# Kernel optimization log

Hardware: AMD Instinct MI355X
Metric: run time of the kernel (lower is better)

The kernel has to match this reference:

```python
import jax, jax.numpy as jnp
import numpy as np

B, T, D = 16, 512, 256          # batch, seq_len, d_model (= num features = num graph nodes N)
H, MC, K, DE, DH = 4, 4, 3, 10, 128
GS, SS, AS = 4, 6, 4            # global/sector/asset regime states
TAU = 0.5
STEPS = 3                       # diffusion steps
HID = max(64, D)
DEC_H = max(64, D // 2)


def setup_inputs() -> dict:
    key = jax.random.key(0)
    ks = iter(jax.random.split(key, 64))

    def nrm(shape, s=0.02):
        return (s * jax.random.normal(next(ks), shape)).astype(jnp.float32)

    z = lambda *s: jnp.zeros(s, jnp.float32)
    o = lambda *s: jnp.ones(s, jnp.float32)
    p = dict(
        x=jax.random.normal(next(ks), (B, T, D), dtype=jnp.float32),
        # hierarchical regime controller
        gW1=nrm((D, HID)), gb1=z(HID), g_ln_w=o(HID), g_ln_b=z(HID),
        gW2=nrm((HID, GS)), gb2=z(GS),
        sW1=nrm((D, HID)), sb1=z(HID), sW2=nrm((HID, D * SS)), sb2=z(D * SS),
        aW1=nrm((D, HID)), ab1=z(HID), aW2=nrm((HID, D * AS)), ab2=z(D * AS),
        global_prior=z(GS), sector_prior=z(SS), asset_prior=z(AS),
        g2f=nrm((GS, D)),
        sector_emb=jax.random.normal(next(ks), (SS, D), dtype=jnp.float32),
        asset_emb=jax.random.normal(next(ks), (AS, D), dtype=jnp.float32),
        # bidirectional temporal scan (BI-Mamba stand-in)
        decay_f=nrm((D,), 1.0), decay_b=nrm((D,), 1.0),
        tW=nrm((D, D)), tb=z(D),
        # Bayesian MAGAC + diffusion graph prior
        psi=nrm((H, D, DE), 0.1), log_sigma=jnp.full((H,), -2.0, jnp.float32),
        step_logits=jnp.linspace(-1.0, 0.5, STEPS).astype(jnp.float32),
        noise_scale=jnp.full((STEPS,), 0.05, jnp.float32),
        Wk=nrm((K + 1, T, DH)),
        mean_w=nrm((DH,)), mean_b=z(), lv_w=nrm((DH,)), lv_b=z(),
        # risk-aware decoder
        dW1=nrm((D, DEC_H)), db1=z(DEC_H), d_ln_w=o(DEC_H), d_ln_b=z(DEC_H),
        mW=nrm((DEC_H,)), mb=z(), lvW=nrm((DEC_H,)), lvb=z(),
        cW=nrm((DEC_H,)), cb=z(),
    )
    return p


def _ln(h, w, b):
    m = h.mean(-1, keepdims=True)
    v = h.var(-1, keepdims=True)  # biased, matches torch LayerNorm
    return (h - m) / jnp.sqrt(v + 1e-5) * w + b


def _gelu(h):
    return jax.nn.gelu(h, approximate=False)


def _gumbel_softmax(k, logits):
    u = jax.random.uniform(k, logits.shape, minval=1e-6, maxval=1.0 - 1e-6)
    g = -jnp.log(-jnp.log(u))
    return jax.nn.softmax((logits + g) / TAU, axis=-1)


def _fwd(x, gW1, gb1, g_ln_w, g_ln_b, gW2, gb2, sW1, sb1, sW2, sb2,
         aW1, ab1, aW2, ab2, global_prior, sector_prior, asset_prior,
         g2f, sector_emb, asset_emb, decay_f, decay_b, tW, tb,
         psi, log_sigma, step_logits, noise_scale, Wk,
         mean_w, mean_b, lv_w, lv_b,
         dW1, db1, d_ln_w, d_ln_b, mW, mb, lvW, lvb, cW, cb):
    rk = jax.random.key(42)
    k_g, k_s, k_a, k_eps, k_diff = jax.random.split(rk, 5)

    # ---- hierarchical regime controller ----
    seq_mean = x.mean(1)                               # (B, D)
    diff_summary = (x[:, 1:] - x[:, :-1]).mean(1)      # (B, D)
    g_logits = _gelu(_ln(seq_mean @ gW1 + gb1, g_ln_w, g_ln_b)) @ gW2 + gb2
    s_logits = (_gelu(seq_mean @ sW1 + sb1) @ sW2 + sb2).reshape(B, D, SS)
    a_logits = (_gelu(diff_summary @ aW1 + ab1) @ aW2 + ab2).reshape(B, D, AS)
    g_probs = _gumbel_softmax(k_g, g_logits)
    s_probs = _gumbel_softmax(k_s, s_logits)
    a_probs = _gumbel_softmax(k_a, a_logits)
    global_gate = g_probs @ g2f                                   # (B, D)
    # diagonal of einsum('bfs,sd->bfd') == einsum('bfs,sf->bf')
    sector_gate = jnp.einsum('bfs,sf->bf', s_probs, sector_emb)
    asset_gate = jnp.einsum('bfs,sf->bf', a_probs, asset_emb)
    feature_gate = jax.nn.sigmoid(global_gate + sector_gate + asset_gate)
    gated_x = x * feature_gate[:, None, :]

    # ---- bidirectional temporal EMA scan (BI-Mamba stand-in) ----
    af = jax.nn.sigmoid(decay_f)
    abk = jax.nn.sigmoid(decay_b)
    xs = gated_x.transpose(1, 0, 2)                    # (T, B, D)

    def ema(a):
        def step(h, xt):
            h = a * h + (1.0 - a) * xt
            return h, h
        return step

    _, hf = jax.lax.scan(ema(af), jnp.zeros_like(xs[0]), xs)
    _, hb = jax.lax.scan(ema(abk), jnp.zeros_like(xs[0]), xs[::-1])
    temporal = (hf + hb[::-1]).transpose(1, 0, 2) @ tW + tb       # (B, T, D)
    node_major = temporal.transpose(0, 2, 1)                      # (B, N=D, T)

    # ---- Bayesian adjacency sampling (MC samples per head) ----
    logits = jnp.einsum('hne,hme->hnm', psi, psi) / jnp.sqrt(jnp.float32(DE))
    sigma = jnp.exp(log_sigma)                                    # (H,)
    eps = jax.random.normal(k_eps, (MC, H, D, D))
    A = jax.nn.softmax(logits[None] + sigma[None, :, None, None] * eps, axis=-1)

    # ---- diffusion refinement guided by regime features ----
    ctx = feature_gate.mean(0)
    ctx = ctx / (jnp.linalg.norm(ctx) + 1e-6)
    outer = ctx[:, None] * ctx[None, :]
    outer = outer / jnp.maximum(outer.sum(-1, keepdims=True), 1e-6)
    dkeys = jax.random.split(k_diff, STEPS)
    for s in range(STEPS):                             # fixed small loop, vectorized over (MC,H)
        alpha = jax.nn.sigmoid(step_logits[s])
        noise = noise_scale[s] * jax.random.normal(dkeys[s], A.shape)
        A = alpha * A + (1.0 - alpha) * outer + noise
        A = 0.5 * (A + jnp.swapaxes(A, -1, -2))
        A = jax.nn.softmax(A, axis=-1)

    # ---- K-hop graph conv, averaged over MC samples and heads ----
    Z = jnp.einsum('bnt,td->bnd', node_major, Wk[0])[None, None]  # hop 0
    P = jnp.broadcast_to(node_major, (MC, H, B, D, T))
    for k in range(1, K + 1):
        P = jnp.einsum('mhnp,mhbpt->mhbnt', A, P)
        Z = Z + jnp.einsum('mhbnt,td->mhbnd', P, Wk[k])
    Z = Z.mean((0, 1))                                            # (B, N, DH)
    graph_mean = Z @ mean_w + mean_b                              # (B, N)
    graph_logvar = Z @ lv_w + lv_b                                # (B, N)

    # ---- risk-aware decoder ----
    feat = _ln(_gelu(graph_mean @ dW1 + db1), d_ln_w, d_ln_b)     # (B, DEC_H)
    mean = feat @ mW + mb
    dec_logvar = feat @ lvW + lvb
    _cvar = jax.nn.sigmoid(feat @ cW + cb)  # auxiliary head (not in returned output)
    var = jnp.exp(dec_logvar) + jnp.exp(graph_logvar).sum(1)
    log_var = jnp.log(var)
    return jnp.stack([mean, log_var], axis=-1)                    # (B, 2)


def reference(x, gW1, gb1, g_ln_w, g_ln_b, gW2, gb2, sW1, sb1, sW2, sb2,
              aW1, ab1, aW2, ab2, global_prior, sector_prior, asset_prior,
              g2f, sector_emb, asset_emb, decay_f, decay_b, tW, tb,
              psi, log_sigma, step_logits, noise_scale, Wk,
              mean_w, mean_b, lv_w, lv_b,
              dW1, db1, d_ln_w, d_ln_b, mW, mb, lvW, lvb, cW, cb):
    return _fwd(x, gW1, gb1, g_ln_w, g_ln_b, gW2, gb2, sW1, sb1, sW2, sb2,
                aW1, ab1, aW2, ab2, global_prior, sector_prior, asset_prior,
                g2f, sector_emb, asset_emb, decay_f, decay_b, tW, tb,
                psi, log_sigma, step_logits, noise_scale, Wk,
                mean_w, mean_b, lv_w, lv_b,
                dW1, db1, d_ln_w, d_ln_b, mW, mb, lvW, lvb, cW, cb)
```

## Files before the change

kernel.cpp:

```cpp
#include <hip/hip_runtime.h>
#include <stdint.h>

#define PARTITIONABLE 1

namespace {

constexpr int GSn = 4, SSn = 6, ASn = 4;

struct TFPair { uint32_t a, b; };

__host__ __device__ constexpr uint32_t rotl32(uint32_t x, int d) {
  return (x << d) | (x >> (32 - d));
}

__host__ __device__ constexpr TFPair tf2x32(uint32_t k0, uint32_t k1,
                                            uint32_t x0, uint32_t x1) {
  uint32_t k2 = k0 ^ k1 ^ 0x1BD11BDAu;
  x0 += k0; x1 += k1;
  x0 += x1; x1 = rotl32(x1, 13); x1 ^= x0;
  x0 += x1; x1 = rotl32(x1, 15); x1 ^= x0;
  x0 += x1; x1 = rotl32(x1, 26); x1 ^= x0;
  x0 += x1; x1 = rotl32(x1, 6);  x1 ^= x0;
  x0 += k1; x1 += k2 + 1u;
  x0 += x1; x1 = rotl32(x1, 17); x1 ^= x0;
  x0 += x1; x1 = rotl32(x1, 29); x1 ^= x0;
  x0 += x1; x1 = rotl32(x1, 16); x1 ^= x0;
  x0 += x1; x1 = rotl32(x1, 24); x1 ^= x0;
  x0 += k2; x1 += k0 + 2u;
  x0 += x1; x1 = rotl32(x1, 13); x1 ^= x0;
  x0 += x1; x1 = rotl32(x1, 15); x1 ^= x0;
  x0 += x1; x1 = rotl32(x1, 26); x1 ^= x0;
  x0 += x1; x1 = rotl32(x1, 6);  x1 ^= x0;
  x0 += k0; x1 += k1 + 3u;
  x0 += x1; x1 = rotl32(x1, 17); x1 ^= x0;
  x0 += x1; x1 = rotl32(x1, 29); x1 ^= x0;
  x0 += x1; x1 = rotl32(x1, 16); x1 ^= x0;
  x0 += x1; x1 = rotl32(x1, 24); x1 ^= x0;
  x0 += k1; x1 += k2 + 4u;
  x0 += x1; x1 = rotl32(x1, 13); x1 ^= x0;
  x0 += x1; x1 = rotl32(x1, 15); x1 ^= x0;
  x0 += x1; x1 = rotl32(x1, 26); x1 ^= x0;
  x0 += x1; x1 = rotl32(x1, 6);  x1 ^= x0;
  x0 += k2; x1 += k0 + 5u;
  return TFPair{x0, x1};
}

#if PARTITIONABLE
constexpr TFPair KG  = tf2x32(0u, 42u, 0u, 0u);
constexpr TFPair KS  = tf2x32(0u, 42u, 0u, 1u);
constexpr TFPair KA  = tf2x32(0u, 42u, 0u, 2u);
constexpr TFPair KE  = tf2x32(0u, 42u, 0u, 3u);
constexpr TFPair KD  = tf2x32(0u, 42u, 0u, 4u);
constexpr TFPair DK0 = tf2x32(KD.a, KD.b, 0u, 0u);
constexpr TFPair DK1 = tf2x32(KD.a, KD.b, 0u, 1u);
constexpr TFPair DK2 = tf2x32(KD.a, KD.b, 0u, 2u);
#else
constexpr TFPair SP0 = tf2x32(0u, 42u, 0u, 5u);
constexpr TFPair SP1 = tf2x32(0u, 42u, 1u, 6u);
constexpr TFPair SP2 = tf2x32(0u, 42u, 2u, 7u);
constexpr TFPair SP3 = tf2x32(0u, 42u, 3u, 8u);
constexpr TFPair SP4 = tf2x32(0u, 42u, 4u, 9u);
constexpr TFPair KG  = TFPair{SP0.a, SP1.a};
constexpr TFPair KS  = TFPair{SP2.a, SP3.a};
constexpr TFPair KA  = TFPair{SP4.a, SP0.b};
constexpr TFPair KE  = TFPair{SP1.b, SP2.b};
constexpr TFPair KD  = TFPair{SP3.b, SP4.b};
constexpr TFPair DP0 = tf2x32(KD.a, KD.b, 0u, 3u);
constexpr TFPair DP1 = tf2x32(KD.a, KD.b, 1u, 4u);
constexpr TFPair DP2 = tf2x32(KD.a, KD.b, 2u, 5u);
constexpr TFPair DK0 = TFPair{DP0.a, DP1.a};
constexpr TFPair DK1 = TFPair{DP2.a, DP0.b};
constexpr TFPair DK2 = TFPair{DP1.b, DP2.b};
#endif

__device__ __forceinline__ uint32_t rbits(uint32_t k0, uint32_t k1,
                                          uint32_t idx, uint32_t half) {
#if PARTITIONABLE
  TFPair t = tf2x32(k0, k1, 0u, idx);
  return t.a ^ t.b;
#else
  if (idx < half) return tf2x32(k0, k1, idx, idx + half).a;
  return tf2x32(k0, k1, idx - half, idx).b;
#endif
}

__device__ __forceinline__ float bits_to_u01(uint32_t bits) {
  return __uint_as_float((bits >> 9) | 0x3F800000u) - 1.0f;
}

__device__ __forceinline__ float gumbel_u(uint32_t k0, uint32_t k1,
                                          uint32_t idx, uint32_t half) {
  const float mn = 1e-6f;
  const float mx = 1.0f - 1e-6f;
  float f = bits_to_u01(rbits(k0, k1, idx, half));
  return fmaxf(mn, f * (mx - mn) + mn);
}

__device__ __forceinline__ float erfinv_f32(float x) {
  float w = -log1pf(-x * x);
  float p;
  if (w < 5.0f) {
    w -= 2.5f;
    p = 2.81022636e-08f;
    p = fmaf(p, w, 3.43273939e-07f);
    p = fmaf(p, w, -3.5233877e-06f);
    p = fmaf(p, w, -4.39150654e-06f);
    p = fmaf(p, w, 0.00021858087f);
    p = fmaf(p, w, -0.00125372503f);
    p = fmaf(p, w, -0.00417768164f);
    p = fmaf(p, w, 0.246640727f);
    p = fmaf(p, w, 1.50140941f);
  } else {
    w = sqrtf(w) - 3.0f;
    p = -0.000200214257f;
    p = fmaf(p, w, 0.000100950558f);
    p = fmaf(p, w, 0.00134934322f);
    p = fmaf(p, w, -0.00367342844f);
    p = fmaf(p, w, 0.00573950773f);
    p = fmaf(p, w, -0.0076224613f);
    p = fmaf(p, w, 0.00943887047f);
    p = fmaf(p, w, 1.00167406f);
    p = fmaf(p, w, 2.83297682f);
  }
  return p * x;
}

__device__ __forceinline__ float normal_from(uint32_t k0, uint32_t k1,
                                             uint32_t idx, uint32_t half) {
  const float lo = -0x1.fffffep-1f;
  float f = bits_to_u01(rbits(k0, k1, idx, half));
  float u = fmaxf(lo, f * 2.0f + lo);
  return 1.41421356237f * erfinv_f32(u);
}

__device__ __forceinline__ float gelu_f(float x) {
  return 0.5f * x * (1.0f + erff(x / 1.4142135623730951f));
}
__device__ __forceinline__ float sigmoid_f(float x) {
  return 1.0f / (1.0f + expf(-x));
}

__device__ __forceinline__ float wave_sum(float v) {
  #pragma unroll
  for (int m = 32; m > 0; m >>= 1) v += __shfl_xor(v, m);
  return v;
}
__device__ __forceinline__ float wave_max(float v) {
  #pragma unroll
  for (int m = 32; m > 0; m >>= 1) v = fmaxf(v, __shfl_xor(v, m));
  return v;
}
template <int NW>
__device__ __forceinline__ float blk_sum(float v, float* slots) {
  v = wave_sum(v);
  int wid = threadIdx.x >> 6;
  if ((threadIdx.x & 63) == 0) slots[wid] = v;
  __syncthreads();
  float r = slots[0];
  #pragma unroll
  for (int i = 1; i < NW; ++i) r += slots[i];
  return r;
}
template <int NW>
__device__ __forceinline__ float blk_max(float v, float* slots) {
  v = wave_max(v);
  int wid = threadIdx.x >> 6;
  if ((threadIdx.x & 63) == 0) slots[wid] = v;
  __syncthreads();
  float r = slots[0];
  #pragma unroll
  for (int i = 1; i < NW; ++i) r = fmaxf(r, slots[i]);
  return r;
}


__global__ __launch_bounds__(256) void k_reduce_x(const float* __restrict__ x,
                                                  float* __restrict__ ps) {
  int blk = blockIdx.x;
  int b = blk >> 4, tc = blk & 15;
  int d = threadIdx.x;
  const float* xp = x + ((size_t)b * 512 + tc * 32) * 256 + d;
  float s = 0.f;
  for (int i = 0; i < 32; ++i) s += xp[(size_t)i * 256];
  ps[(size_t)blk * 256 + d] = s;
}

__global__ void k_combine(const float* __restrict__ x,
                          const float* __restrict__ ps, float* __restrict__ sm,
                          float* __restrict__ ds) {
  int b = blockIdx.x, d = threadIdx.x;
  float s = 0.f;
  for (int tc = 0; tc < 16; ++tc) s += ps[(size_t)(b * 16 + tc) * 256 + d];
  sm[b * 256 + d] = s / 512.0f;
  const float* xb = x + (size_t)b * 512 * 256 + d;
  ds[b * 256 + d] = (xb[(size_t)511 * 256] - xb[0]) / 511.0f;
}

__global__ __launch_bounds__(256) void k_hidden(
    const float* __restrict__ sm, const float* __restrict__ ds,
    const float* __restrict__ gW1, const float* __restrict__ gb1,
    const float* __restrict__ glnw, const float* __restrict__ glnb,
    const float* __restrict__ sW1, const float* __restrict__ sb1,
    const float* __restrict__ aW1, const float* __restrict__ ab1,
    float* __restrict__ hgG, float* __restrict__ hgS,
    float* __restrict__ hgA) {
  __shared__ float inv[256];
  __shared__ float s1[4], s2[4];
  int head = blockIdx.x >> 4, b = blockIdx.x & 15, j = threadIdx.x;
  const float* in = (head == 2) ? ds : sm;
  const float* W1 = (head == 0) ? gW1 : (head == 1) ? sW1 : aW1;
  const float* b1 = (head == 0) ? gb1 : (head == 1) ? sb1 : ab1;
  inv[j] = in[b * 256 + j];
  __syncthreads();
  float h = b1[j];
  for (int d = 0; d < 256; ++d) h = fmaf(inv[d], W1[d * 256 + j], h);
  float* outp = (head == 0) ? hgG : (head == 1) ? hgS : hgA;
  if (head == 0) {
    float mean = blk_sum<4>(h, s1) / 256.0f;
    float dv = h - mean;
    float var = blk_sum<4>(dv * dv, s2) / 256.0f;
    h = dv / sqrtf(var + 1e-5f) * glnw[j] + glnb[j];
  }
  outp[b * 256 + j] = gelu_f(h);
}

__global__ __launch_bounds__(192) void k_s2(const float* __restrict__ hgS,
                                            const float* __restrict__ sW2,
                                            const float* __restrict__ sb2,
                                            const float* __restrict__ semb,
                                            float* __restrict__ sgate) {
  __shared__ float hs[256];
  __shared__ float lv[32][6];
  int b = blockIdx.x, f0 = blockIdx.y * 32;
  int tid = threadIdx.x;
  int fl = tid / 6, s = tid - fl * 6;
  for (int i = tid; i < 256; i += 192) hs[i] = hgS[b * 256 + i];
  __syncthreads();
  int f = f0 + fl;
  const float* wcol = sW2 + f * 6 + s;
  float acc = sb2[f * 6 + s];
  for (int d = 0; d < 256; ++d) acc = fmaf(hs[d], wcol[(size_t)d * 1536], acc);
  float u = gumbel_u(KS.a, KS.b, (uint32_t)(b * 256 + f) * 6u + s, 12288u);
  float g = -logf(-logf(u));
  lv[fl][s] = (acc + g) / 0.5f;
  __syncthreads();
  if (tid < 32) {
    int ff = f0 + tid;
    float v0 = lv[tid][0], v1 = lv[tid][1], v2 = lv[tid][2];
    float v3 = lv[tid][3], v4 = lv[tid][4], v5 = lv[tid][5];
    float mx = fmaxf(fmaxf(fmaxf(v0, v1), fmaxf(v2, v3)), fmaxf(v4, v5));
    float e0 = expf(v0 - mx), e1 = expf(v1 - mx), e2 = expf(v2 - mx);
    float e3 = expf(v3 - mx), e4 = expf(v4 - mx), e5 = expf(v5 - mx);
    float sum = e0 + e1 + e2 + e3 + e4 + e5;
    float sg = (e0 * semb[0 * 256 + ff] + e1 * semb[1 * 256 + ff] +
                e2 * semb[2 * 256 + ff] + e3 * semb[3 * 256 + ff] +
                e4 * semb[4 * 256 + ff] + e5 * semb[5 * 256 + ff]) / sum;
    sgate[b * 256 + ff] = sg;
  }
}

__global__ __launch_bounds__(256) void k_a2(const float* __restrict__ hgA,
                                            const float* __restrict__ aW2,
                                            const float* __restrict__ ab2,
                                            const float* __restrict__ aemb,
                                            float* __restrict__ agate) {
  __shared__ float hs[256];
  __shared__ float lv[64][4];
  int b = blockIdx.x, f0 = blockIdx.y * 64;
  int tid = threadIdx.x;
  int fl = tid >> 2, s = tid & 3;
  hs[tid] = hgA[b * 256 + tid];
  __syncthreads();
  int f = f0 + fl;
  const float* wcol = aW2 + f * 4 + s;
  float acc = ab2[f * 4 + s];
  for (int d = 0; d < 256; ++d) acc = fmaf(hs[d], wcol[(size_t)d * 1024], acc);
  float u = gumbel_u(KA.a, KA.b, (uint32_t)(b * 256 + f) * 4u + s, 8192u);
  float g = -logf(-logf(u));
  lv[fl][s] = (acc + g) / 0.5f;
  __syncthreads();
  if (tid < 64) {
    int ff = f0 + tid;
    float v0 = lv[tid][0], v1 = lv[tid][1], v2 = lv[tid][2], v3 = lv[tid][3];
    float mx = fmaxf(fmaxf(v0, v1), fmaxf(v2, v3));
    float e0 = expf(v0 - mx), e1 = expf(v1 - mx);
    float e2 = expf(v2 - mx), e3 = expf(v3 - mx);
    float sum = e0 + e1 + e2 + e3;
    float ag = (e0 * aemb[0 * 256 + ff] + e1 * aemb[1 * 256 + ff] +
                e2 * aemb[2 * 256 + ff] + e3 * aemb[3 * 256 + ff]) / sum;
    agate[b * 256 + ff] = ag;
  }
}

__global__ __launch_bounds__(256) void k_fgate(
    const float* __restrict__ hgG, const float* __restrict__ gW2,
    const float* __restrict__ gb2, const float* __restrict__ g2f,
    const float* __restrict__ sgate, const float* __restrict__ agate,
    float* __restrict__ fg) {
  __shared__ float slots[4][4];
  __shared__ float vals[4];
  __shared__ float gp[4];
  int b = blockIdx.x, j = threadIdx.x;
  float hj = hgG[b * 256 + j];
  float lg[4];
  #pragma unroll
  for (int s = 0; s < 4; ++s)
    lg[s] = blk_sum<4>(hj * gW2[j * 4 + s], slots[s]);
  if (j < 4) {
    float u = gumbel_u(KG.a, KG.b, (uint32_t)(b * 4 + j), 32u);
    float g = -logf(-logf(u));
    vals[j] = (lg[j] + gb2[j] + g) / 0.5f;
  }
  __syncthreads();
  if (j < 4) {
    float mx = fmaxf(fmaxf(vals[0], vals[1]), fmaxf(vals[2], vals[3]));
    float sum = expf(vals[0] - mx) + expf(vals[1] - mx) + expf(vals[2] - mx) +
                expf(vals[3] - mx);
    gp[j] = expf(vals[j] - mx) / sum;
  }
  __syncthreads();
  int f = j;
  float gg = 0.f;
  #pragma unroll
  for (int s = 0; s < 4; ++s) gg = fmaf(gp[s], g2f[s * 256 + f], gg);
  fg[b * 256 + f] = sigmoid_f(gg + sgate[b * 256 + f] + agate[b * 256 + f]);
}

__global__ __launch_bounds__(256) void k_ctx(const float* __restrict__ fg,
                                             float* __restrict__ ctx) {
  __shared__ float s1[4], s2[4];
  int f = threadIdx.x;
  float c = 0.f;
  for (int b = 0; b < 16; ++b) c += fg[b * 256 + f];
  c /= 16.0f;
  float ss = blk_sum<4>(c * c, s1);
  float cv = c / (sqrtf(ss) + 1e-6f);
  ctx[f] = cv;
  float S = blk_sum<4>(cv, s2);
  if (f == 0) ctx[256] = S;
}

__global__ __launch_bounds__(256) void k_vcompute(const float* __restrict__ Wk,
                                                  const float* __restrict__ mean_w,
                                                  const float* __restrict__ lv_w,
                                                  float* __restrict__ v,
                                                  float* __restrict__ sv) {
  int j = blockIdx.x >> 2, tg = blockIdx.x & 3;
  const float* wp = (j & 1) ? lv_w : mean_w;
  const float* Wkk = Wk + (size_t)(j >> 1) * 65536;
  int wid = threadIdx.x >> 6, lane = threadIdx.x & 63;
  float w0 = wp[lane], w1 = wp[64 + lane];
  float svloc = 0.f;
  for (int i = 0; i < 32; ++i) {
    int t = tg * 128 + wid * 32 + i;
    const float* row = Wkk + (size_t)t * 128;
    float s = row[lane] * w0 + row[64 + lane] * w1;
    s = wave_sum(s);
    if (lane == 0) { v[j * 512 + t] = s; svloc += s; }
  }
  if (lane == 0) atomicAdd(&sv[j], svloc);
}

__global__ __launch_bounds__(256) void k_scan1(
    const float* __restrict__ x, const float* __restrict__ fg,
    const float* __restrict__ decay_f, const float* __restrict__ decay_b,
    const float* __restrict__ v, float* __restrict__ Pf, float* __restrict__ Qf,
    float* __restrict__ Pb, float* __restrict__ Qb, float* __restrict__ Lf,
    float* __restrict__ Lb) {
  __shared__ float vv[8][32];
  int blk = blockIdx.x;
  int b = blk >> 4, c = blk & 15;
  int d = threadIdx.x;
  { int j = d >> 5, i = d & 31; vv[j][i] = v[j * 512 + c * 32 + i]; }
  __syncthreads();
  float g = fg[b * 256 + d];
  float af = sigmoid_f(decay_f[d]);
  float ab = sigmoid_f(decay_b[d]);
  float r_gx[32];
  const float* xp = x + ((size_t)b * 512 + c * 32) * 256 + d;
  #pragma unroll
  for (int i = 0; i < 32; ++i) r_gx[i] = xp[(size_t)i * 256] * g;
  float h = 0.f, pw = 1.f;
  float P[8], Q[8];
  #pragma unroll
  for (int j = 0; j < 8; ++j) { P[j] = 0.f; Q[j] = 0.f; }
  #pragma unroll
  for (int i = 0; i < 32; ++i) {
    h = fmaf(af, h, (1.0f - af) * r_gx[i]);
    pw *= af;
    #pragma unroll
    for (int j = 0; j < 8; ++j) {
      float vj = vv[j][i];
      P[j] = fmaf(h, vj, P[j]);
      Q[j] = fmaf(pw, vj, Q[j]);
    }
  }
  size_t base = ((size_t)(b * 16 + c) * 8) * 256 + d;
  #pragma unroll
  for (int j = 0; j < 8; ++j) { Pf[base + j * 256] = P[j]; Qf[base + j * 256] = Q[j]; }
  Lf[(b * 16 + c) * 256 + d] = h;
  h = 0.f; pw = 1.f;
  #pragma unroll
  for (int j = 0; j < 8; ++j) { P[j] = 0.f; Q[j] = 0.f; }
  #pragma unroll
  for (int i = 31; i >= 0; --i) {
    h = fmaf(ab, h, (1.0f - ab) * r_gx[i]);
    pw *= ab;
    #pragma unroll
    for (int j = 0; j < 8; ++j) {
      float vj = vv[j][i];
      P[j] = fmaf(h, vj, P[j]);
      Q[j] = fmaf(pw, vj, Q[j]);
    }
  }
  #pragma unroll
  for (int j = 0; j < 8; ++j) { Pb[base + j * 256] = P[j]; Qb[base + j * 256] = Q[j]; }
  Lb[(b * 16 + c) * 256 + d] = h;
}

__global__ __launch_bounds__(256) void k_scan2(
    const float* __restrict__ Pf, const float* __restrict__ Qf,
    const float* __restrict__ Pb, const float* __restrict__ Qb,
    const float* __restrict__ Lf, const float* __restrict__ Lb,
    const float* __restrict__ decay_f, const float* __restrict__ decay_b,
    float* __restrict__ u) {
  int blk = blockIdx.x;
  int b = blk >> 3, j = blk & 7;
  int d = threadIdx.x;
  float af = sigmoid_f(decay_f[d]);
  float ab = sigmoid_f(decay_b[d]);
  float af32 = af, ab32 = ab;
  #pragma unroll
  for (int q = 0; q < 5; ++q) { af32 *= af32; ab32 *= ab32; }
  float acc = 0.f, H = 0.f;
  for (int c = 0; c < 16; ++c) {
    size_t base = ((size_t)(b * 16 + c) * 8 + j) * 256 + d;
    acc += Pf[base] + H * Qf[base];
    H = Lf[(b * 16 + c) * 256 + d] + af32 * H;
  }
  H = 0.f;
  for (int c = 15; c >= 0; --c) {
    size_t base = ((size_t)(b * 16 + c) * 8 + j) * 256 + d;
    acc += Pb[base] + H * Qb[base];
    H = Lb[(b * 16 + c) * 256 + d] + ab32 * H;
  }
  u[(b * 8 + j) * 256 + d] = acc;
}

__global__ __launch_bounds__(256) void k_ygemm(
    const float* __restrict__ u, const float* __restrict__ tW,
    const float* __restrict__ tb, const float* __restrict__ sv,
    const float* __restrict__ mean_b, const float* __restrict__ lv_b,
    float* __restrict__ gm, float* __restrict__ glv, float* __restrict__ YH) {
  __shared__ float As[32][33];
  __shared__ float Bs[32][33];
  __shared__ float svs[8];
  int n0 = blockIdx.x * 32, m0 = blockIdx.y * 32;
  int tid = threadIdx.x, tx = tid & 31, ty = tid >> 5;
  if (tid < 8) svs[tid] = sv[tid];
  float acc[4] = {0.f, 0.f, 0.f, 0.f};
  for (int k0 = 0; k0 < 256; k0 += 32) {
    #pragma unroll
    for (int l = 0; l < 4; ++l) {
      int e = tid + l * 256, r = e >> 5, cc = e & 31;
      As[r][cc] = u[(size_t)(m0 + r) * 256 + k0 + cc];
      Bs[r][cc] = tW[(size_t)(k0 + r) * 256 + n0 + cc];
    }
    __syncthreads();
    #pragma unroll
    for (int kk = 0; kk < 32; ++kk) {
      float bv = Bs[kk][tx];
      #pragma unroll
      for (int i = 0; i < 4; ++i) acc[i] = fmaf(As[ty + 8 * i][kk], bv, acc[i]);
    }
    __syncthreads();
  }
  int n = n0 + tx;
  float tbn = tb[n];
  float mb0 = mean_b[0], lb0 = lv_b[0];
  #pragma unroll
  for (int i = 0; i < 4; ++i) {
    int row = m0 + ty + 8 * i;
    int b = row >> 3, j = row & 7;
    float val = acc[i] + tbn * svs[j];
    if (j == 0) gm[b * 256 + n] = val + mb0;
    else if (j == 1) glv[b * 256 + n] = val + lb0;
    else {
      int k = (j >> 1) - 1, proj = j & 1;
      YH[k * 8192 + n * 32 + b * 2 + proj] = val;
    }
  }
}

__global__ __launch_bounds__(256) void k_a_init(const float* __restrict__ psi,
                                                const float* __restrict__ log_sigma,
                                                float* __restrict__ A) {
  __shared__ float pn[12];
  __shared__ float s1[4], s2[4];
  int blk = blockIdx.x;
  int mh = blk >> 8, h = mh & 3, n = blk & 255, p = threadIdx.x;
  if (p < 10) pn[p] = psi[(size_t)(h * 256 + n) * 10 + p];
  __syncthreads();
  const float* pp = psi + (size_t)(h * 256 + p) * 10;
  float s = 0.f;
  #pragma unroll
  for (int e = 0; e < 10; ++e) s = fmaf(pn[e], pp[e], s);
  float logit = s / sqrtf(10.0f);
  uint32_t idx = (uint32_t)blk * 256u + (uint32_t)p;
  float eps = normal_from(KE.a, KE.b, idx, 524288u);
  float val = logit + expf(log_sigma[h]) * eps;
  float mx = blk_max<4>(val, s1);
  float e = expf(val - mx);
  float sum = blk_sum<4>(e, s2);
  A[(size_t)blk * 256 + p] = e / sum;
}

__global__ __launch_bounds__(256) void k_mix_sym(
    const float* __restrict__ Ain, float* __restrict__ Aout,
    const float* __restrict__ ctx, const float* __restrict__ step_logits,
    const float* __restrict__ noise_scale, int s, uint32_t dk0, uint32_t dk1) {
  __shared__ float s1[4], s2[4];
  int blk = blockIdx.x;
  int mh = blk >> 8, n = blk & 255, p = threadIdx.x;
  float alpha = sigmoid_f(step_logits[s]);
  float ns = noise_scale[s];
  float cn = ctx[n], cp = ctx[p], S = ctx[256];
  float o_np = (cn * cp) / fmaxf(cn * S, 1e-6f);
  float o_pn = (cp * cn) / fmaxf(cp * S, 1e-6f);
  uint32_t i_np = (uint32_t)blk * 256u + (uint32_t)p;
  uint32_t i_pn = (uint32_t)mh * 65536u + (uint32_t)p * 256u + (uint32_t)n;
  float a_np = Ain[(size_t)mh * 65536 + n * 256 + p];
  float a_pn = Ain[(size_t)mh * 65536 + p * 256 + n];
  float m_np = alpha * a_np + (1.0f - alpha) * o_np +
               ns * normal_from(dk0, dk1, i_np, 524288u);
  float m_pn = alpha * a_pn + (1.0f - alpha) * o_pn +
               ns * normal_from(dk0, dk1, i_pn, 524288u);
  float val = 0.5f * (m_np + m_pn);
  float mx = blk_max<4>(val, s1);
  float e = expf(val - mx);
  float sum = blk_sum<4>(e, s2);
  Aout[(size_t)blk * 256 + p] = e / sum;
}

__global__ __launch_bounds__(256) void k_horner(
    const float* __restrict__ A, const float* __restrict__ Rin, int sRin,
    const float* __restrict__ Yadd, float* __restrict__ Rout) {
  int nt = blockIdx.x, mh = blockIdx.y;
  int n0 = nt * 32;
  __shared__ float As[32][33];
  __shared__ float Bs[32][33];
  int tid = threadIdx.x, tx = tid & 31, ty = tid >> 5;
  float acc[4] = {0.f, 0.f, 0.f, 0.f};
  const float* Ab = A + (size_t)mh * 65536;
  const float* Rb = Rin + (size_t)mh * sRin;
  for (int k0 = 0; k0 < 256; k0 += 32) {
    #pragma unroll
    for (int l = 0; l < 4; ++l) {
      int e = tid + l * 256, r = e >> 5, cc = e & 31;
      As[r][cc] = Ab[(size_t)(n0 + r) * 256 + k0 + cc];
      Bs[r][cc] = Rb[(size_t)(k0 + r) * 32 + cc];
    }
    __syncthreads();
    #pragma unroll
    for (int kk = 0; kk < 32; ++kk) {
      float bv = Bs[kk][tx];
      #pragma unroll
      for (int i = 0; i < 4; ++i) acc[i] = fmaf(As[ty + 8 * i][kk], bv, acc[i]);
    }
    __syncthreads();
  }
  #pragma unroll
  for (int i = 0; i < 4; ++i) {
    int n = n0 + ty + 8 * i;
    float vv = acc[i];
    if (Yadd) vv += Yadd[n * 32 + tx];
    Rout[(size_t)mh * 8192 + (size_t)n * 32 + tx] = vv;
  }
}

__global__ void k_final(const float* __restrict__ R, float* __restrict__ gm,
                        float* __restrict__ glv) {
  int b = blockIdx.x, n = threadIdx.x;
  float sm_ = 0.f, sl = 0.f;
  for (int mh = 0; mh < 16; ++mh) {
    sm_ += R[(size_t)mh * 8192 + n * 32 + b * 2];
    sl += R[(size_t)mh * 8192 + n * 32 + b * 2 + 1];
  }
  gm[b * 256 + n] += sm_ * (1.0f / 16.0f);
  glv[b * 256 + n] += sl * (1.0f / 16.0f);
}

__global__ __launch_bounds__(128) void k_decoder(
    const float* __restrict__ gm, const float* __restrict__ glv,
    const float* __restrict__ dW1, const float* __restrict__ db1,
    const float* __restrict__ dlnw, const float* __restrict__ dlnb,
    const float* __restrict__ mW, const float* __restrict__ mb,
    const float* __restrict__ lvW, const float* __restrict__ lvb,
    float* __restrict__ out) {
  __shared__ float gmv[256];
  __shared__ float s1[2], s2[2], s3[2], s4[2], s5[2];
  int b = blockIdx.x, j = threadIdx.x;
  gmv[j] = gm[b * 256 + j];
  gmv[j + 128] = gm[b * 256 + j + 128];
  __syncthreads();
  float h = db1[j];
  for (int n = 0; n < 256; ++n) h = fmaf(gmv[n], dW1[n * 128 + j], h);
  h = gelu_f(h);
  float mean = blk_sum<2>(h, s1) / 128.0f;
  float dv = h - mean;
  float var = blk_sum<2>(dv * dv, s2) / 128.0f;
  float feat = dv / sqrtf(var + 1e-5f) * dlnw[j] + dlnb[j];
  float m_c = blk_sum<2>(feat * mW[j], s3) + mb[0];
  float lv_c = blk_sum<2>(feat * lvW[j], s4) + lvb[0];
  float se = expf(glv[b * 256 + j]) + expf(glv[b * 256 + j + 128]);
  float sumexp = blk_sum<2>(se, s5);
  if (j == 0) {
    out[b * 2 + 0] = m_c;
    out[b * 2 + 1] = logf(expf(lv_c) + sumexp);
  }
}

constexpr size_t O_SM = 0;
constexpr size_t O_DS = 4096;
constexpr size_t O_PS = 8192;
constexpr size_t O_HGG = 73728;
constexpr size_t O_HGS = 77824;
constexpr size_t O_HGA = 81920;
constexpr size_t O_SG = 86016;
constexpr size_t O_AG = 90112;
constexpr size_t O_FG = 94208;
constexpr size_t O_CTX = 98304;
constexpr size_t O_V = 98624;
constexpr size_t O_SV = 102720;
constexpr size_t O_U = 102784;
constexpr size_t O_PF = 135552;
constexpr size_t O_QF = 659840;
constexpr size_t O_PB = 1184128;
constexpr size_t O_QB = 1708416;
constexpr size_t O_LF = 2232704;
constexpr size_t O_LB = 2298240;
constexpr size_t O_YH = 2363776;
constexpr size_t O_R1 = 2388352;
constexpr size_t O_R2 = 2519424;
constexpr size_t O_GM = 2650496;
constexpr size_t O_GLV = 2654592;
constexpr size_t O_A = 2658688;
constexpr size_t O_A2 = 3707264;

}

extern "C" void kernel_launch(void* const* d_in, const int* in_sizes, int n_in,
                              void* d_out, int out_size, void* d_ws,
                              size_t ws_size, hipStream_t stream) {
  (void)in_sizes; (void)n_in; (void)out_size; (void)ws_size;
  const float* x = (const float*)d_in[0];
  const float* gW1 = (const float*)d_in[1];
  const float* gb1 = (const float*)d_in[2];
  const float* g_ln_w = (const float*)d_in[3];
  const float* g_ln_b = (const float*)d_in[4];
  const float* gW2 = (const float*)d_in[5];
  const float* gb2 = (const float*)d_in[6];
  const float* sW1 = (const float*)d_in[7];
  const float* sb1 = (const float*)d_in[8];
  const float* sW2 = (const float*)d_in[9];
  const float* sb2 = (const float*)d_in[10];
  const float* aW1 = (const float*)d_in[11];
  const float* ab1 = (const float*)d_in[12];
  const float* aW2 = (const float*)d_in[13];
  const float* ab2 = (const float*)d_in[14];
  const float* g2f = (const float*)d_in[18];
  const float* sector_emb = (const float*)d_in[19];
  const float* asset_emb = (const float*)d_in[20];
  const float* decay_f = (const float*)d_in[21];
  const float* decay_b = (const float*)d_in[22];
  const float* tW = (const float*)d_in[23];
  const float* tb = (const float*)d_in[24];
  const float* psi = (const float*)d_in[25];
  const float* log_sigma = (const float*)d_in[26];
  const float* step_logits = (const float*)d_in[27];
  const float* noise_scale = (const float*)d_in[28];
  const float* Wk = (const float*)d_in[29];
  const float* mean_w = (const float*)d_in[30];
  const float* mean_b = (const float*)d_in[31];
  const float* lv_w = (const float*)d_in[32];
  const float* lv_b = (const float*)d_in[33];
  const float* dW1 = (const float*)d_in[34];
  const float* db1 = (const float*)d_in[35];
  const float* d_ln_w = (const float*)d_in[36];
  const float* d_ln_b = (const float*)d_in[37];
  const float* mW = (const float*)d_in[38];
  const float* mb = (const float*)d_in[39];
  const float* lvW = (const float*)d_in[40];
  const float* lvb = (const float*)d_in[41];
  float* out = (float*)d_out;
  float* w = (float*)d_ws;

  const uint32_t dka[3] = {DK0.a, DK1.a, DK2.a};
  const uint32_t dkb[3] = {DK0.b, DK1.b, DK2.b};

  hipMemsetAsync(w + O_SV, 0, 64 * sizeof(float), stream);

  k_reduce_x<<<256, 256, 0, stream>>>(x, w + O_PS);
  k_combine<<<16, 256, 0, stream>>>(x, w + O_PS, w + O_SM, w + O_DS);
  k_hidden<<<48, 256, 0, stream>>>(w + O_SM, w + O_DS, gW1, gb1, g_ln_w,
                                   g_ln_b, sW1, sb1, aW1, ab1, w + O_HGG,
                                   w + O_HGS, w + O_HGA);
  k_s2<<<dim3(16, 8), 192, 0, stream>>>(w + O_HGS, sW2, sb2, sector_emb,
                                        w + O_SG);
  k_a2<<<dim3(16, 4), 256, 0, stream>>>(w + O_HGA, aW2, ab2, asset_emb,
                                        w + O_AG);
  k_fgate<<<16, 256, 0, stream>>>(w + O_HGG, gW2, gb2, g2f, w + O_SG, w + O_AG,
                                  w + O_FG);
  k_ctx<<<1, 256, 0, stream>>>(w + O_FG, w + O_CTX);

  k_a_init<<<4096, 256, 0, stream>>>(psi, log_sigma, w + O_A);
  const size_t asrc[3] = {O_A, O_A2, O_A};
  const size_t adst[3] = {O_A2, O_A, O_A2};
  for (int s = 0; s < 3; ++s) {
    k_mix_sym<<<4096, 256, 0, stream>>>(w + asrc[s], w + adst[s], w + O_CTX,
                                        step_logits, noise_scale, s, dka[s],
                                        dkb[s]);
  }

  k_vcompute<<<32, 256, 0, stream>>>(Wk, mean_w, lv_w, w + O_V, w + O_SV);
  k_scan1<<<256, 256, 0, stream>>>(x, w + O_FG, decay_f, decay_b, w + O_V,
                                   w + O_PF, w + O_QF, w + O_PB, w + O_QB,
                                   w + O_LF, w + O_LB);
  k_scan2<<<128, 256, 0, stream>>>(w + O_PF, w + O_QF, w + O_PB, w + O_QB,
                                   w + O_LF, w + O_LB, decay_f, decay_b,
                                   w + O_U);
  k_ygemm<<<dim3(8, 4), 256, 0, stream>>>(w + O_U, tW, tb, w + O_SV, mean_b,
                                          lv_b, w + O_GM, w + O_GLV, w + O_YH);

  k_horner<<<dim3(8, 16), 256, 0, stream>>>(w + O_A2, w + O_YH + 2 * 8192, 0,
                                            w + O_YH + 1 * 8192, w + O_R1);
  k_horner<<<dim3(8, 16), 256, 0, stream>>>(w + O_A2, w + O_R1, 8192, w + O_YH,
                                            w + O_R2);
  k_horner<<<dim3(8, 16), 256, 0, stream>>>(w + O_A2, w + O_R2, 8192, nullptr,
                                            w + O_R1);
  k_final<<<16, 256, 0, stream>>>(w + O_R1, w + O_GM, w + O_GLV);

  k_decoder<<<16, 128, 0, stream>>>(w + O_GM, w + O_GLV, dW1, db1, d_ln_w,
                                    d_ln_b, mW, mb, lvW, lvb, out);
}
```

Measured before the change: 358.6 us.

## Fuse many small kernels into phased launches with heterogeneous block roles

Restructures the pipeline from about twenty launches into eleven kernels. Each kernel runs several independent phases, chosen by block index (e.g. hidden layer alongside A-init, gates fused with sector/asset heads), and all pointers are passed in a single Params struct. This targets launch overhead and the idle GPU time in tiny serial kernels by overlapping independent work within one grid. The cost is more complex block-to-phase mapping, and possibly more registers or shared memory per kernel.

```diff
diff --git a/kernel.cpp b/kernel.cpp
--- a/kernel.cpp
+++ b/kernel.cpp
@@ -4,8 +4,6 @@
 #define PARTITIONABLE 1
 
 namespace {
-
-constexpr int GSn = 4, SSn = 6, ASn = 4;
 
 struct TFPair { uint32_t a, b; };
 
@@ -173,182 +171,53 @@
   return r;
 }
 
-
-__global__ __launch_bounds__(256) void k_reduce_x(const float* __restrict__ x,
-                                                  float* __restrict__ ps) {
-  int blk = blockIdx.x;
-  int b = blk >> 4, tc = blk & 15;
-  int d = threadIdx.x;
-  const float* xp = x + ((size_t)b * 512 + tc * 32) * 256 + d;
-  float s = 0.f;
-  for (int i = 0; i < 32; ++i) s += xp[(size_t)i * 256];
-  ps[(size_t)blk * 256 + d] = s;
-}
-
-__global__ void k_combine(const float* __restrict__ x,
-                          const float* __restrict__ ps, float* __restrict__ sm,
-                          float* __restrict__ ds) {
-  int b = blockIdx.x, d = threadIdx.x;
-  float s = 0.f;
-  for (int tc = 0; tc < 16; ++tc) s += ps[(size_t)(b * 16 + tc) * 256 + d];
-  sm[b * 256 + d] = s / 512.0f;
-  const float* xb = x + (size_t)b * 512 * 256 + d;
-  ds[b * 256 + d] = (xb[(size_t)511 * 256] - xb[0]) / 511.0f;
-}
-
-__global__ __launch_bounds__(256) void k_hidden(
-    const float* __restrict__ sm, const float* __restrict__ ds,
-    const float* __restrict__ gW1, const float* __restrict__ gb1,
-    const float* __restrict__ glnw, const float* __restrict__ glnb,
-    const float* __restrict__ sW1, const float* __restrict__ sb1,
-    const float* __restrict__ aW1, const float* __restrict__ ab1,
-    float* __restrict__ hgG, float* __restrict__ hgS,
-    float* __restrict__ hgA) {
-  __shared__ float inv[256];
-  __shared__ float s1[4], s2[4];
-  int head = blockIdx.x >> 4, b = blockIdx.x & 15, j = threadIdx.x;
-  const float* in = (head == 2) ? ds : sm;
-  const float* W1 = (head == 0) ? gW1 : (head == 1) ? sW1 : aW1;
-  const float* b1 = (head == 0) ? gb1 : (head == 1) ? sb1 : ab1;
-  inv[j] = in[b * 256 + j];
+struct Params {
+  const float *x, *gW1, *gb1, *glnw, *glnb, *gW2, *gb2, *sW1, *sb1, *sW2, *sb2,
+      *aW1, *ab1, *aW2, *ab2, *g2f, *semb, *aemb, *decay_f, *decay_b, *tW, *tb,
+      *psi, *log_sigma, *step_logits, *noise_scale, *Wk, *mean_w, *mean_b,
+      *lv_w, *lv_b, *dW1, *db1, *dlnw, *dlnb, *mW, *mb, *lvW, *lvb;
+  float* out;
+  float *ps, *ds, *hgG, *hgS, *hgA, *fg, *ctx, *v, *sv, *u, *Pf, *Qf, *Pb, *Qb,
+      *Lf, *Lb, *YH, *R1, *R2, *gm, *glv, *A, *A2;
+};
+
+
+__device__ __forceinline__ void phase_hidden(const Params& P, float* smem,
+                                             int bid, int tid) {
+  float* inv = smem;
+  float* s1 = smem + 256;
+  float* s2 = smem + 260;
+  int head = bid >> 4, b = bid & 15;
+  float iv;
+  if (head < 2) {
+    float s = 0.f;
+    for (int tc = 0; tc < 16; ++tc) s += P.ps[(size_t)(b * 16 + tc) * 256 + tid];
+    iv = s / 512.0f;
+  } else {
+    iv = P.ds[b * 256 + tid];
+  }
+  inv[tid] = iv;
   __syncthreads();
-  float h = b1[j];
-  for (int d = 0; d < 256; ++d) h = fmaf(inv[d], W1[d * 256 + j], h);
-  float* outp = (head == 0) ? hgG : (head == 1) ? hgS : hgA;
+  const float* W1 = (head == 0) ? P.gW1 : (head == 1) ? P.sW1 : P.aW1;
+  const float* b1 = (head == 0) ? P.gb1 : (head == 1) ? P.sb1 : P.ab1;
+  float h = b1[tid];
+  for (int d = 0; d < 256; ++d) h = fmaf(inv[d], W1[d * 256 + tid], h);
   if (head == 0) {
     float mean = blk_sum<4>(h, s1) / 256.0f;
     float dv = h - mean;
     float var = blk_sum<4>(dv * dv, s2) / 256.0f;
-    h = dv / sqrtf(var + 1e-5f) * glnw[j] + glnb[j];
-  }
-  outp[b * 256 + j] = gelu_f(h);
-}
-
-__global__ __launch_bounds__(192) void k_s2(const float* __restrict__ hgS,
-                                            const float* __restrict__ sW2,
-                                            const float* __restrict__ sb2,
-                                            const float* __restrict__ semb,
-                                            float* __restrict__ sgate) {
-  __shared__ float hs[256];
-  __shared__ float lv[32][6];
-  int b = blockIdx.x, f0 = blockIdx.y * 32;
-  int tid = threadIdx.x;
-  int fl = tid / 6, s = tid - fl * 6;
-  for (int i = tid; i < 256; i += 192) hs[i] = hgS[b * 256 + i];
-  __syncthreads();
-  int f = f0 + fl;
-  const float* wcol = sW2 + f * 6 + s;
-  float acc = sb2[f * 6 + s];
-  for (int d = 0; d < 256; ++d) acc = fmaf(hs[d], wcol[(size_t)d * 1536], acc);
-  float u = gumbel_u(KS.a, KS.b, (uint32_t)(b * 256 + f) * 6u + s, 12288u);
-  float g = -logf(-logf(u));
-  lv[fl][s] = (acc + g) / 0.5f;
-  __syncthreads();
-  if (tid < 32) {
-    int ff = f0 + tid;
-    float v0 = lv[tid][0], v1 = lv[tid][1], v2 = lv[tid][2];
-    float v3 = lv[tid][3], v4 = lv[tid][4], v5 = lv[tid][5];
-    float mx = fmaxf(fmaxf(fmaxf(v0, v1), fmaxf(v2, v3)), fmaxf(v4, v5));
-    float e0 = expf(v0 - mx), e1 = expf(v1 - mx), e2 = expf(v2 - mx);
-    float e3 = expf(v3 - mx), e4 = expf(v4 - mx), e5 = expf(v5 - mx);
-    float sum = e0 + e1 + e2 + e3 + e4 + e5;
-    float sg = (e0 * semb[0 * 256 + ff] + e1 * semb[1 * 256 + ff] +
-                e2 * semb[2 * 256 + ff] + e3 * semb[3 * 256 + ff] +
-                e4 * semb[4 * 256 + ff] + e5 * semb[5 * 256 + ff]) / sum;
-    sgate[b * 256 + ff] = sg;
-  }
-}
-
-__global__ __launch_bounds__(256) void k_a2(const float* __restrict__ hgA,
-                                            const float* __restrict__ aW2,
-                                            const float* __restrict__ ab2,
-                                            const float* __restrict__ aemb,
-                                            float* __restrict__ agate) {
-  __shared__ float hs[256];
-  __shared__ float lv[64][4];
-  int b = blockIdx.x, f0 = blockIdx.y * 64;
-  int tid = threadIdx.x;
-  int fl = tid >> 2, s = tid & 3;
-  hs[tid] = hgA[b * 256 + tid];
-  __syncthreads();
-  int f = f0 + fl;
-  const float* wcol = aW2 + f * 4 + s;
-  float acc = ab2[f * 4 + s];
-  for (int d = 0; d < 256; ++d) acc = fmaf(hs[d], wcol[(size_t)d * 1024], acc);
-  float u = gumbel_u(KA.a, KA.b, (uint32_t)(b * 256 + f) * 4u + s, 8192u);
-  float g = -logf(-logf(u));
-  lv[fl][s] = (acc + g) / 0.5f;
-  __syncthreads();
-  if (tid < 64) {
-    int ff = f0 + tid;
-    float v0 = lv[tid][0], v1 = lv[tid][1], v2 = lv[tid][2], v3 = lv[tid][3];
-    float mx = fmaxf(fmaxf(v0, v1), fmaxf(v2, v3));
-    float e0 = expf(v0 - mx), e1 = expf(v1 - mx);
-    float e2 = expf(v2 - mx), e3 = expf(v3 - mx);
-    float sum = e0 + e1 + e2 + e3;
-    float ag = (e0 * aemb[0 * 256 + ff] + e1 * aemb[1 * 256 + ff] +
-                e2 * aemb[2 * 256 + ff] + e3 * aemb[3 * 256 + ff]) / sum;
-    agate[b * 256 + ff] = ag;
-  }
-}
-
-__global__ __launch_bounds__(256) void k_fgate(
-    const float* __restrict__ hgG, const float* __restrict__ gW2,
-    const float* __restrict__ gb2, const float* __restrict__ g2f,
-    const float* __restrict__ sgate, const float* __restrict__ agate,
-    float* __restrict__ fg) {
-  __shared__ float slots[4][4];
-  __shared__ float vals[4];
-  __shared__ float gp[4];
-  int b = blockIdx.x, j = threadIdx.x;
-  float hj = hgG[b * 256 + j];
-  float lg[4];
-  #pragma unroll
-  for (int s = 0; s < 4; ++s)
-    lg[s] = blk_sum<4>(hj * gW2[j * 4 + s], slots[s]);
-  if (j < 4) {
-    float u = gumbel_u(KG.a, KG.b, (uint32_t)(b * 4 + j), 32u);
-    float g = -logf(-logf(u));
-    vals[j] = (lg[j] + gb2[j] + g) / 0.5f;
-  }
-  __syncthreads();
-  if (j < 4) {
-    float mx = fmaxf(fmaxf(vals[0], vals[1]), fmaxf(vals[2], vals[3]));
-    float sum = expf(vals[0] - mx) + expf(vals[1] - mx) + expf(vals[2] - mx) +
-                expf(vals[3] - mx);
-    gp[j] = expf(vals[j] - mx) / sum;
-  }
-  __syncthreads();
-  int f = j;
-  float gg = 0.f;
-  #pragma unroll
-  for (int s = 0; s < 4; ++s) gg = fmaf(gp[s], g2f[s * 256 + f], gg);
-  fg[b * 256 + f] = sigmoid_f(gg + sgate[b * 256 + f] + agate[b * 256 + f]);
-}
-
-__global__ __launch_bounds__(256) void k_ctx(const float* __restrict__ fg,
-                                             float* __restrict__ ctx) {
-  __shared__ float s1[4], s2[4];
-  int f = threadIdx.x;
-  float c = 0.f;
-  for (int b = 0; b < 16; ++b) c += fg[b * 256 + f];
-  c /= 16.0f;
-  float ss = blk_sum<4>(c * c, s1);
-  float cv = c / (sqrtf(ss) + 1e-6f);
-  ctx[f] = cv;
-  float S = blk_sum<4>(cv, s2);
-  if (f == 0) ctx[256] = S;
-}
-
-__global__ __launch_bounds__(256) void k_vcompute(const float* __restrict__ Wk,
-                                                  const float* __restrict__ mean_w,
-                                                  const float* __restrict__ lv_w,
-                                                  float* __restrict__ v,
-                                                  float* __restrict__ sv) {
-  int j = blockIdx.x >> 2, tg = blockIdx.x & 3;
-  const float* wp = (j & 1) ? lv_w : mean_w;
-  const float* Wkk = Wk + (size_t)(j >> 1) * 65536;
-  int wid = threadIdx.x >> 6, lane = threadIdx.x & 63;
+    h = dv / sqrtf(var + 1e-5f) * P.glnw[tid] + P.glnb[tid];
+  }
+  float* outp = (head == 0) ? P.hgG : (head == 1) ? P.hgS : P.hgA;
+  outp[b * 256 + tid] = gelu_f(h);
+}
+
+__device__ __forceinline__ void phase_vcompute(const Params& P, int bid2,
+                                               int tid) {
+  int j = bid2 >> 2, tg = bid2 & 3;
+  const float* wp = (j & 1) ? P.lv_w : P.mean_w;
+  const float* Wkk = P.Wk + (size_t)(j >> 1) * 65536;
+  int wid = tid >> 6, lane = tid & 63;
   float w0 = wp[lane], w1 = wp[64 + lane];
   float svloc = 0.f;
   for (int i = 0; i < 32; ++i) {
@@ -356,200 +225,303 @@
     const float* row = Wkk + (size_t)t * 128;
     float s = row[lane] * w0 + row[64 + lane] * w1;
     s = wave_sum(s);
-    if (lane == 0) { v[j * 512 + t] = s; svloc += s; }
-  }
-  if (lane == 0) atomicAdd(&sv[j], svloc);
-}
-
-__global__ __launch_bounds__(256) void k_scan1(
-    const float* __restrict__ x, const float* __restrict__ fg,
-    const float* __restrict__ decay_f, const float* __restrict__ decay_b,
-    const float* __restrict__ v, float* __restrict__ Pf, float* __restrict__ Qf,
-    float* __restrict__ Pb, float* __restrict__ Qb, float* __restrict__ Lf,
-    float* __restrict__ Lb) {
-  __shared__ float vv[8][32];
-  int blk = blockIdx.x;
-  int b = blk >> 4, c = blk & 15;
-  int d = threadIdx.x;
-  { int j = d >> 5, i = d & 31; vv[j][i] = v[j * 512 + c * 32 + i]; }
+    if (lane == 0) { P.v[j * 512 + t] = s; svloc += s; }
+  }
+  if (lane == 0) atomicAdd(&P.sv[j], svloc);
+}
+
+__device__ __forceinline__ void phase_ainit(const Params& P, float* smem,
+                                            int row0, int nrows, int tid) {
+  float* pn = smem;
+  float* s1 = smem + 12;
+  float* s2 = smem + 16;
+  for (int r = 0; r < nrows; ++r) {
+    int blk = row0 + r;
+    int mh = blk >> 8, h = mh & 3, n = blk & 255, p = tid;
+    if (p < 10) pn[p] = P.psi[(size_t)(h * 256 + n) * 10 + p];
+    __syncthreads();
+    const float* pp = P.psi + (size_t)(h * 256 + p) * 10;
+    float s = 0.f;
+    #pragma unroll
+    for (int e = 0; e < 10; ++e) s = fmaf(pn[e], pp[e], s);
+    float logit = s / sqrtf(10.0f);
+    uint32_t idx = (uint32_t)blk * 256u + (uint32_t)p;
+    float eps = normal_from(KE.a, KE.b, idx, 524288u);
+    float val = logit + expf(P.log_sigma[h]) * eps;
+    float mx = blk_max<4>(val, s1);
+    float e = expf(val - mx);
+    float sum = blk_sum<4>(e, s2);
+    P.A[(size_t)blk * 256 + p] = e / sum;
+  }
+}
+
+__device__ __forceinline__ void phase_gates(const Params& P, float* smem,
+                                            int bid, int tid) {
+  float* hgGs = smem;
+  float* hgSs = smem + 256;
+  float* hgAs = smem + 512;
+  float* lvS = smem + 768;
+  float* lvA = smem + 1152;
+  float* gsl = smem + 1408;
+  float* gvals = smem + 1424;
+  float* gpv = smem + 1428;
+  int b = bid >> 2, f0 = (bid & 3) * 64;
+  hgGs[tid] = P.hgG[b * 256 + tid];
+  hgSs[tid] = P.hgS[b * 256 + tid];
+  hgAs[tid] = P.hgA[b * 256 + tid];
   __syncthreads();
-  float g = fg[b * 256 + d];
-  float af = sigmoid_f(decay_f[d]);
-  float ab = sigmoid_f(decay_b[d]);
+  float lg[4];
+  #pragma unroll
+  for (int s = 0; s < 4; ++s)
+    lg[s] = blk_sum<4>(hgGs[tid] * P.gW2[tid * 4 + s], gsl + 4 * s);
+  if (tid < 4) {
+    float u = gumbel_u(KG.a, KG.b, (uint32_t)(b * 4 + tid), 32u);
+    float g = -logf(-logf(u));
+    gvals[tid] = (lg[tid] + P.gb2[tid] + g) / 0.5f;
+  }
+  __syncthreads();
+  if (tid < 4) {
+    float mx = fmaxf(fmaxf(gvals[0], gvals[1]), fmaxf(gvals[2], gvals[3]));
+    float sum = expf(gvals[0] - mx) + expf(gvals[1] - mx) +
+                expf(gvals[2] - mx) + expf(gvals[3] - mx);
+    gpv[tid] = expf(gvals[tid] - mx) / sum;
+  }
+  {
+    int o = tid;
+    int fl = o / 6, s = o - fl * 6;
+    int f = f0 + fl;
+    const float* wp = P.sW2 + f * 6 + s;
+    float acc = P.sb2[f * 6 + s];
+    for (int d = 0; d < 256; ++d) acc = fmaf(hgSs[d], wp[(size_t)d * 1536], acc);
+    float u = gumbel_u(KS.a, KS.b, (uint32_t)(b * 256 + f) * 6u + s, 12288u);
+    lvS[o] = (acc + (-logf(-logf(u)))) / 0.5f;
+  }
+  if (tid < 128) {
+    int o = tid + 256;
+    int fl = o / 6, s = o - fl * 6;
+    int f = f0 + fl;
+    const float* wp = P.sW2 + f * 6 + s;
+    float acc = P.sb2[f * 6 + s];
+    for (int d = 0; d < 256; ++d) acc = fmaf(hgSs[d], wp[(size_t)d * 1536], acc);
+    float u = gumbel_u(KS.a, KS.b, (uint32_t)(b * 256 + f) * 6u + s, 12288u);
+    lvS[o] = (acc + (-logf(-logf(u)))) / 0.5f;
+  }
+  {
+    int fl = tid >> 2, s = tid & 3;
+    int f = f0 + fl;
+    const float* wp = P.aW2 + f * 4 + s;
+    float acc = P.ab2[f * 4 + s];
+    for (int d = 0; d < 256; ++d) acc = fmaf(hgAs[d], wp[(size_t)d * 1024], acc);
+    float u = gumbel_u(KA.a, KA.b, (uint32_t)(b * 256 + f) * 4u + s, 8192u);
+    lvA[tid] = (acc + (-logf(-logf(u)))) / 0.5f;
+  }
+  __syncthreads();
+  if (tid < 64) {
+    int f = f0 + tid;
+    float v0 = lvS[tid * 6 + 0], v1 = lvS[tid * 6 + 1], v2 = lvS[tid * 6 + 2];
+    float v3 = lvS[tid * 6 + 3], v4 = lvS[tid * 6 + 4], v5 = lvS[tid * 6 + 5];
+    float mx = fmaxf(fmaxf(fmaxf(v0, v1), fmaxf(v2, v3)), fmaxf(v4, v5));
+    float e0 = expf(v0 - mx), e1 = expf(v1 - mx), e2 = expf(v2 - mx);
+    float e3 = expf(v3 - mx), e4 = expf(v4 - mx), e5 = expf(v5 - mx);
+    float ssum = e0 + e1 + e2 + e3 + e4 + e5;
+    float sg = (e0 / ssum) * P.semb[0 * 256 + f] + (e1 / ssum) * P.semb[1 * 256 + f] +
+               (e2 / ssum) * P.semb[2 * 256 + f] + (e3 / ssum) * P.semb[3 * 256 + f] +
+               (e4 / ssum) * P.semb[4 * 256 + f] + (e5 / ssum) * P.semb[5 * 256 + f];
+    float a0 = lvA[tid * 4 + 0], a1 = lvA[tid * 4 + 1];
+    float a2 = lvA[tid * 4 + 2], a3 = lvA[tid * 4 + 3];
+    float amx = fmaxf(fmaxf(a0, a1), fmaxf(a2, a3));
+    float x0 = expf(a0 - amx), x1 = expf(a1 - amx);
+    float x2 = expf(a2 - amx), x3 = expf(a3 - amx);
+    float asum = x0 + x1 + x2 + x3;
+    float ag = (x0 / asum) * P.aemb[0 * 256 + f] + (x1 / asum) * P.aemb[1 * 256 + f] +
+               (x2 / asum) * P.aemb[2 * 256 + f] + (x3 / asum) * P.aemb[3 * 256 + f];
+    float gg = 0.f;
+    #pragma unroll
+    for (int s = 0; s < 4; ++s) gg = fmaf(gpv[s], P.g2f[s * 256 + f], gg);
+    P.fg[b * 256 + f] = sigmoid_f(gg + sg + ag);
+  }
+}
+
+__device__ __forceinline__ void phase_ctx(const Params& P, float* smem,
+                                          int tid) {
+  float* s1 = smem;
+  float* s2 = smem + 4;
+  float c = 0.f;
+  for (int b = 0; b < 16; ++b) c += P.fg[b * 256 + tid];
+  c /= 16.0f;
+  float ss = blk_sum<4>(c * c, s1);
+  float cv = c / (sqrtf(ss) + 1e-6f);
+  P.ctx[tid] = cv;
+  float S = blk_sum<4>(cv, s2);
+  if (tid == 0) P.ctx[256] = S;
+}
+
+__device__ __forceinline__ void phase_scan1(const Params& P, float* smem,
+                                            int ch, int tid) {
+  float* vv = smem;
+  int b = ch >> 4, c = ch & 15;
+  int d = tid;
+  vv[(d >> 5) * 32 + (d & 31)] = P.v[(d >> 5) * 512 + c * 32 + (d & 31)];
+  __syncthreads();
+  float g = P.fg[b * 256 + d];
+  float af = sigmoid_f(P.decay_f[d]);
+  float ab = sigmoid_f(P.decay_b[d]);
   float r_gx[32];
-  const float* xp = x + ((size_t)b * 512 + c * 32) * 256 + d;
+  const float* xp = P.x + ((size_t)b * 512 + c * 32) * 256 + d;
   #pragma unroll
   for (int i = 0; i < 32; ++i) r_gx[i] = xp[(size_t)i * 256] * g;
   float h = 0.f, pw = 1.f;
-  float P[8], Q[8];
-  #pragma unroll
-  for (int j = 0; j < 8; ++j) { P[j] = 0.f; Q[j] = 0.f; }
+  float Pr[8], Q[8];
+  #pragma unroll
+  for (int j = 0; j < 8; ++j) { Pr[j] = 0.f; Q[j] = 0.f; }
   #pragma unroll
   for (int i = 0; i < 32; ++i) {
     h = fmaf(af, h, (1.0f - af) * r_gx[i]);
     pw *= af;
     #pragma unroll
     for (int j = 0; j < 8; ++j) {
-      float vj = vv[j][i];
-      P[j] = fmaf(h, vj, P[j]);
+      float vj = vv[j * 32 + i];
+      Pr[j] = fmaf(h, vj, Pr[j]);
       Q[j] = fmaf(pw, vj, Q[j]);
     }
   }
   size_t base = ((size_t)(b * 16 + c) * 8) * 256 + d;
   #pragma unroll
-  for (int j = 0; j < 8; ++j) { Pf[base + j * 256] = P[j]; Qf[base + j * 256] = Q[j]; }
-  Lf[(b * 16 + c) * 256 + d] = h;
+  for (int j = 0; j < 8; ++j) {
+    P.Pf[base + j * 256] = Pr[j];
+    P.Qf[base + j * 256] = Q[j];
+  }
+  P.Lf[(b * 16 + c) * 256 + d] = h;
   h = 0.f; pw = 1.f;
   #pragma unroll
-  for (int j = 0; j < 8; ++j) { P[j] = 0.f; Q[j] = 0.f; }
+  for (int j = 0; j < 8; ++j) { Pr[j] = 0.f; Q[j] = 0.f; }
   #pragma unroll
   for (int i = 31; i >= 0; --i) {
     h = fmaf(ab, h, (1.0f - ab) * r_gx[i]);
     pw *= ab;
     #pragma unroll
     for (int j = 0; j < 8; ++j) {
-      float vj = vv[j][i];
-      P[j] = fmaf(h, vj, P[j]);
+      float vj = vv[j * 32 + i];
+      Pr[j] = fmaf(h, vj, Pr[j]);
       Q[j] = fmaf(pw, vj, Q[j]);
     }
   }
   #pragma unroll
-  for (int j = 0; j < 8; ++j) { Pb[base + j * 256] = P[j]; Qb[base + j * 256] = Q[j]; }
-  Lb[(b * 16 + c) * 256 + d] = h;
-}
-
-__global__ __launch_bounds__(256) void k_scan2(
-    const float* __restrict__ Pf, const float* __restrict__ Qf,
-    const float* __restrict__ Pb, const float* __restrict__ Qb,
-    const float* __restrict__ Lf, const float* __restrict__ Lb,
-    const float* __restrict__ decay_f, const float* __restrict__ decay_b,
-    float* __restrict__ u) {
-  int blk = blockIdx.x;
+  for (int j = 0; j < 8; ++j) {
+    P.Pb[base + j * 256] = Pr[j];
+    P.Qb[base + j * 256] = Q[j];
+  }
+  P.Lb[(b * 16 + c) * 256 + d] = h;
+}
+
+__device__ __forceinline__ void phase_scan2(const Params& P, int blk, int tid) {
   int b = blk >> 3, j = blk & 7;
-  int d = threadIdx.x;
-  float af = sigmoid_f(decay_f[d]);
-  float ab = sigmoid_f(decay_b[d]);
+  int d = tid;
+  float af = sigmoid_f(P.decay_f[d]);
+  float ab = sigmoid_f(P.decay_b[d]);
   float af32 = af, ab32 = ab;
   #pragma unroll
   for (int q = 0; q < 5; ++q) { af32 *= af32; ab32 *= ab32; }
   float acc = 0.f, H = 0.f;
   for (int c = 0; c < 16; ++c) {
     size_t base = ((size_t)(b * 16 + c) * 8 + j) * 256 + d;
-    acc += Pf[base] + H * Qf[base];
-    H = Lf[(b * 16 + c) * 256 + d] + af32 * H;
+    acc += P.Pf[base] + H * P.Qf[base];
+    H = P.Lf[(b * 16 + c) * 256 + d] + af32 * H;
   }
   H = 0.f;
   for (int c = 15; c >= 0; --c) {
     size_t base = ((size_t)(b * 16 + c) * 8 + j) * 256 + d;
-    acc += Pb[base] + H * Qb[base];
-    H = Lb[(b * 16 + c) * 256 + d] + ab32 * H;
-  }
-  u[(b * 8 + j) * 256 + d] = acc;
-}
-
-__global__ __launch_bounds__(256) void k_ygemm(
-    const float* __restrict__ u, const float* __restrict__ tW,
-    const float* __restrict__ tb, const float* __restrict__ sv,
-    const float* __restrict__ mean_b, const float* __restrict__ lv_b,
-    float* __restrict__ gm, float* __restrict__ glv, float* __restrict__ YH) {
-  __shared__ float As[32][33];
-  __shared__ float Bs[32][33];
-  __shared__ float svs[8];
-  int n0 = blockIdx.x * 32, m0 = blockIdx.y * 32;
-  int tid = threadIdx.x, tx = tid & 31, ty = tid >> 5;
-  if (tid < 8) svs[tid] = sv[tid];
+    acc += P.Pb[base] + H * P.Qb[base];
+    H = P.Lb[(b * 16 + c) * 256 + d] + ab32 * H;
+  }
+  P.u[(b * 8 + j) * 256 + d] = acc;
+}
+
+__device__ __forceinline__ void phase_ygemm(const Params& P, float* smem,
+                                            int blk32, int tid) {
+  float* As = smem;
+  float* Bs = smem + 1056;
+  float* svs = smem + 2112;
+  int n0 = (blk32 & 7) * 32, m0 = (blk32 >> 3) * 32;
+  int tx = tid & 31, ty = tid >> 5;
+  if (tid < 8) svs[tid] = P.sv[tid];
   float acc[4] = {0.f, 0.f, 0.f, 0.f};
   for (int k0 = 0; k0 < 256; k0 += 32) {
     #pragma unroll
     for (int l = 0; l < 4; ++l) {
       int e = tid + l * 256, r = e >> 5, cc = e & 31;
-      As[r][cc] = u[(size_t)(m0 + r) * 256 + k0 + cc];
-      Bs[r][cc] = tW[(size_t)(k0 + r) * 256 + n0 + cc];
+      As[r * 33 + cc] = P.u[(size_t)(m0 + r) * 256 + k0 + cc];
+      Bs[r * 33 + cc] = P.tW[(size_t)(k0 + r) * 256 + n0 + cc];
     }
     __syncthreads();
     #pragma unroll
     for (int kk = 0; kk < 32; ++kk) {
-      float bv = Bs[kk][tx];
+      float bv = Bs[kk * 33 + tx];
       #pragma unroll
-      for (int i = 0; i < 4; ++i) acc[i] = fmaf(As[ty + 8 * i][kk], bv, acc[i]);
+      for (int i = 0; i < 4; ++i)
+        acc[i] = fmaf(As[(ty + 8 * i) * 33 + kk], bv, acc[i]);
     }
     __syncthreads();
   }
   int n = n0 + tx;
-  float tbn = tb[n];
-  float mb0 = mean_b[0], lb0 = lv_b[0];
+  float tbn = P.tb[n];
+  float mb0 = P.mean_b[0], lb0 = P.lv_b[0];
   #pragma unroll
   for (int i = 0; i < 4; ++i) {
     int row = m0 + ty + 8 * i;
     int b = row >> 3, j = row & 7;
     float val = acc[i] + tbn * svs[j];
-    if (j == 0) gm[b * 256 + n] = val + mb0;
-    else if (j == 1) glv[b * 256 + n] = val + lb0;
+    if (j == 0) P.gm[b * 256 + n] = val + mb0;
+    else if (j == 1) P.glv[b * 256 + n] = val + lb0;
     else {
       int k = (j >> 1) - 1, proj = j & 1;
-      YH[k * 8192 + n * 32 + b * 2 + proj] = val;
+      P.YH[k * 8192 + n * 32 + b * 2 + proj] = val;
     }
   }
 }
 
-__global__ __launch_bounds__(256) void k_a_init(const float* __restrict__ psi,
-                                                const float* __restrict__ log_sigma,
-                                                float* __restrict__ A) {
-  __shared__ float pn[12];
-  __shared__ float s1[4], s2[4];
-  int blk = blockIdx.x;
-  int mh = blk >> 8, h = mh & 3, n = blk & 255, p = threadIdx.x;
-  if (p < 10) pn[p] = psi[(size_t)(h * 256 + n) * 10 + p];
-  __syncthreads();
-  const float* pp = psi + (size_t)(h * 256 + p) * 10;
-  float s = 0.f;
-  #pragma unroll
-  for (int e = 0; e < 10; ++e) s = fmaf(pn[e], pp[e], s);
-  float logit = s / sqrtf(10.0f);
-  uint32_t idx = (uint32_t)blk * 256u + (uint32_t)p;
-  float eps = normal_from(KE.a, KE.b, idx, 524288u);
-  float val = logit + expf(log_sigma[h]) * eps;
-  float mx = blk_max<4>(val, s1);
-  float e = expf(val - mx);
-  float sum = blk_sum<4>(e, s2);
-  A[(size_t)blk * 256 + p] = e / sum;
-}
-
-__global__ __launch_bounds__(256) void k_mix_sym(
-    const float* __restrict__ Ain, float* __restrict__ Aout,
-    const float* __restrict__ ctx, const float* __restrict__ step_logits,
-    const float* __restrict__ noise_scale, int s, uint32_t dk0, uint32_t dk1) {
-  __shared__ float s1[4], s2[4];
-  int blk = blockIdx.x;
-  int mh = blk >> 8, n = blk & 255, p = threadIdx.x;
-  float alpha = sigmoid_f(step_logits[s]);
-  float ns = noise_scale[s];
-  float cn = ctx[n], cp = ctx[p], S = ctx[256];
-  float o_np = (cn * cp) / fmaxf(cn * S, 1e-6f);
-  float o_pn = (cp * cn) / fmaxf(cp * S, 1e-6f);
-  uint32_t i_np = (uint32_t)blk * 256u + (uint32_t)p;
-  uint32_t i_pn = (uint32_t)mh * 65536u + (uint32_t)p * 256u + (uint32_t)n;
-  float a_np = Ain[(size_t)mh * 65536 + n * 256 + p];
-  float a_pn = Ain[(size_t)mh * 65536 + p * 256 + n];
-  float m_np = alpha * a_np + (1.0f - alpha) * o_np +
-               ns * normal_from(dk0, dk1, i_np, 524288u);
-  float m_pn = alpha * a_pn + (1.0f - alpha) * o_pn +
-               ns * normal_from(dk0, dk1, i_pn, 524288u);
-  float val = 0.5f * (m_np + m_pn);
-  float mx = blk_max<4>(val, s1);
-  float e = expf(val - mx);
-  float sum = blk_sum<4>(e, s2);
-  Aout[(size_t)blk * 256 + p] = e / sum;
-}
-
-__global__ __launch_bounds__(256) void k_horner(
-    const float* __restrict__ A, const float* __restrict__ Rin, int sRin,
-    const float* __restrict__ Yadd, float* __restrict__ Rout) {
-  int nt = blockIdx.x, mh = blockIdx.y;
+__device__ __forceinline__ void phase_mix(const Params& P, float* smem,
+                                          int sidx, const float* Ain,
+                                          float* Aout, uint32_t dk0,
+                                          uint32_t dk1, int row0, int nrows,
+                                          int tid) {
+  float* s1 = smem;
+  float* s2 = smem + 4;
+  float alpha = sigmoid_f(P.step_logits[sidx]);
+  float ns = P.noise_scale[sidx];
+  float S = P.ctx[256];
+  float cp = P.ctx[tid];
+  for (int i = 0; i < nrows; ++i) {
+    int blk = row0 + i;
+    int mh = blk >> 8, n = blk & 255, p = tid;
+    float cn = P.ctx[n];
+    float o_np = (cn * cp) / fmaxf(cn * S, 1e-6f);
+    float o_pn = (cp * cn) / fmaxf(cp * S, 1e-6f);
+    uint32_t i_np = (uint32_t)blk * 256u + (uint32_t)p;
+    uint32_t i_pn = (uint32_t)mh * 65536u + (uint32_t)p * 256u + (uint32_t)n;
+    float a_np = Ain[(size_t)mh * 65536 + n * 256 + p];
+    float a_pn = Ain[(size_t)mh * 65536 + p * 256 + n];
+    float m_np = alpha * a_np + (1.0f - alpha) * o_np +
+                 ns * normal_from(dk0, dk1, i_np, 524288u);
+    float m_pn = alpha * a_pn + (1.0f - alpha) * o_pn +
+                 ns * normal_from(dk0, dk1, i_pn, 524288u);
+    float val = 0.5f * (m_np + m_pn);
+    float mx = blk_max<4>(val, s1);
+    float e = expf(val - mx);
+    float sum = blk_sum<4>(e, s2);
+    Aout[(size_t)blk * 256 + p] = e / sum;
+  }
+}
+
+__device__ __forceinline__ void phase_horner(const Params& P, float* smem,
+                                             const float* A, const float* Rin,
+                                             int sRin, const float* Yadd,
+                                             float* Rout, int bid, int tid) {
+  float* As = smem;
+  float* Bs = smem + 1056;
+  int nt = bid & 7, mh = bid >> 3;
   int n0 = nt * 32;
-  __shared__ float As[32][33];
-  __shared__ float Bs[32][33];
-  int tid = threadIdx.x, tx = tid & 31, ty = tid >> 5;
+  int tx = tid & 31, ty = tid >> 5;
   float acc[4] = {0.f, 0.f, 0.f, 0.f};
   const float* Ab = A + (size_t)mh * 65536;
   const float* Rb = Rin + (size_t)mh * sRin;
@@ -557,15 +529,16 @@
     #pragma unroll
     for (int l = 0; l < 4; ++l) {
       int e = tid + l * 256, r = e >> 5, cc = e & 31;
-      As[r][cc] = Ab[(size_t)(n0 + r) * 256 + k0 + cc];
-      Bs[r][cc] = Rb[(size_t)(k0 + r) * 32 + cc];
+      As[r * 33 + cc] = Ab[(size_t)(n0 + r) * 256 + k0 + cc];
+      Bs[r * 33 + cc] = Rb[(size_t)(k0 + r) * 32 + cc];
     }
     __syncthreads();
     #pragma unroll
     for (int kk = 0; kk < 32; ++kk) {
-      float bv = Bs[kk][tx];
+      float bv = Bs[kk * 33 + tx];
       #pragma unroll
-      for (int i = 0; i < 4; ++i) acc[i] = fmaf(As[ty + 8 * i][kk], bv, acc[i]);
+      for (int i = 0; i < 4; ++i)
+        acc[i] = fmaf(As[(ty + 8 * i) * 33 + kk], bv, acc[i]);
     }
     __syncthreads();
   }
@@ -578,74 +551,140 @@
   }
 }
 
-__global__ void k_final(const float* __restrict__ R, float* __restrict__ gm,
-                        float* __restrict__ glv) {
-  int b = blockIdx.x, n = threadIdx.x;
-  float sm_ = 0.f, sl = 0.f;
+__device__ __forceinline__ void phase_findec(const Params& P, float* smem,
+                                             int bid, int tid) {
+  float* gmv = smem;
+  float* sl = smem + 256;
+  int b = bid;
+  float sm_ = 0.f, sl_ = 0.f;
   for (int mh = 0; mh < 16; ++mh) {
-    sm_ += R[(size_t)mh * 8192 + n * 32 + b * 2];
-    sl += R[(size_t)mh * 8192 + n * 32 + b * 2 + 1];
-  }
-  gm[b * 256 + n] += sm_ * (1.0f / 16.0f);
-  glv[b * 256 + n] += sl * (1.0f / 16.0f);
-}
-
-__global__ __launch_bounds__(128) void k_decoder(
-    const float* __restrict__ gm, const float* __restrict__ glv,
-    const float* __restrict__ dW1, const float* __restrict__ db1,
-    const float* __restrict__ dlnw, const float* __restrict__ dlnb,
-    const float* __restrict__ mW, const float* __restrict__ mb,
-    const float* __restrict__ lvW, const float* __restrict__ lvb,
-    float* __restrict__ out) {
-  __shared__ float gmv[256];
-  __shared__ float s1[2], s2[2], s3[2], s4[2], s5[2];
-  int b = blockIdx.x, j = threadIdx.x;
-  gmv[j] = gm[b * 256 + j];
-  gmv[j + 128] = gm[b * 256 + j + 128];
+    sm_ += P.R1[(size_t)mh * 8192 + tid * 32 + b * 2];
+    sl_ += P.R1[(size_t)mh * 8192 + tid * 32 + b * 2 + 1];
+  }
+  float gmn = P.gm[b * 256 + tid] + sm_ * (1.0f / 16.0f);
+  float gln = P.glv[b * 256 + tid] + sl_ * (1.0f / 16.0f);
+  gmv[tid] = gmn;
+  float se = expf(gln);
   __syncthreads();
-  float h = db1[j];
-  for (int n = 0; n < 256; ++n) h = fmaf(gmv[n], dW1[n * 128 + j], h);
-  h = gelu_f(h);
-  float mean = blk_sum<2>(h, s1) / 128.0f;
-  float dv = h - mean;
-  float var = blk_sum<2>(dv * dv, s2) / 128.0f;
-  float feat = dv / sqrtf(var + 1e-5f) * dlnw[j] + dlnb[j];
-  float m_c = blk_sum<2>(feat * mW[j], s3) + mb[0];
-  float lv_c = blk_sum<2>(feat * lvW[j], s4) + lvb[0];
-  float se = expf(glv[b * 256 + j]) + expf(glv[b * 256 + j + 128]);
-  float sumexp = blk_sum<2>(se, s5);
-  if (j == 0) {
-    out[b * 2 + 0] = m_c;
-    out[b * 2 + 1] = logf(expf(lv_c) + sumexp);
-  }
-}
-
-constexpr size_t O_SM = 0;
-constexpr size_t O_DS = 4096;
-constexpr size_t O_PS = 8192;
-constexpr size_t O_HGG = 73728;
-constexpr size_t O_HGS = 77824;
-constexpr size_t O_HGA = 81920;
-constexpr size_t O_SG = 86016;
-constexpr size_t O_AG = 90112;
-constexpr size_t O_FG = 94208;
-constexpr size_t O_CTX = 98304;
-constexpr size_t O_V = 98624;
-constexpr size_t O_SV = 102720;
-constexpr size_t O_U = 102784;
-constexpr size_t O_PF = 135552;
-constexpr size_t O_QF = 659840;
-constexpr size_t O_PB = 1184128;
-constexpr size_t O_QB = 1708416;
-constexpr size_t O_LF = 2232704;
-constexpr size_t O_LB = 2298240;
-constexpr size_t O_YH = 2363776;
-constexpr size_t O_R1 = 2388352;
-constexpr size_t O_R2 = 2519424;
-constexpr size_t O_GM = 2650496;
-constexpr size_t O_GLV = 2654592;
-constexpr size_t O_A = 2658688;
-constexpr size_t O_A2 = 3707264;
+  float sumexp = blk_sum<4>(se, sl);
+  float h = 0.f;
+  if (tid < 128) {
+    h = P.db1[tid];
+    for (int n = 0; n < 256; ++n) h = fmaf(gmv[n], P.dW1[n * 128 + tid], h);
+    h = gelu_f(h);
+  }
+  float mean = blk_sum<4>(tid < 128 ? h : 0.f, sl + 4) / 128.0f;
+  float dv = (tid < 128) ? h - mean : 0.f;
+  float var = blk_sum<4>(dv * dv, sl + 8) / 128.0f;
+  float feat = (tid < 128) ? dv / sqrtf(var + 1e-5f) * P.dlnw[tid] + P.dlnb[tid]
+                           : 0.f;
+  float m_c = blk_sum<4>(tid < 128 ? feat * P.mW[tid] : 0.f, sl + 12) + P.mb[0];
+  float lv_c = blk_sum<4>(tid < 128 ? feat * P.lvW[tid] : 0.f, sl + 16) + P.lvb[0];
+  if (tid == 0) {
+    P.out[b * 2 + 0] = m_c;
+    P.out[b * 2 + 1] = logf(expf(lv_c) + sumexp);
+  }
+}
+
+
+__global__ __launch_bounds__(256) void kL0(Params P) {
+  int bid = blockIdx.x, tid = threadIdx.x;
+  int b = bid >> 4, tc = bid & 15;
+  const float* xp = P.x + ((size_t)b * 512 + tc * 32) * 256 + tid;
+  float s = 0.f;
+  for (int i = 0; i < 32; ++i) s += xp[(size_t)i * 256];
+  P.ps[(size_t)bid * 256 + tid] = s;
+  if (tc == 0) {
+    const float* xb = P.x + (size_t)b * 512 * 256 + tid;
+    P.ds[b * 256 + tid] = (xb[(size_t)511 * 256] - xb[0]) / 511.0f;
+  }
+}
+
+__global__ __launch_bounds__(256) void kL1(Params P) {
+  __shared__ float smem[272];
+  int bid = blockIdx.x, tid = threadIdx.x;
+  if (bid < 48) phase_hidden(P, smem, bid, tid);
+  else if (bid < 80) phase_vcompute(P, bid - 48, tid);
+  else phase_ainit(P, smem, (bid - 80) * 16, 16, tid);
+}
+
+__global__ __launch_bounds__(256) void kL2(Params P) {
+  __shared__ float smem[1440];
+  int bid = blockIdx.x, tid = threadIdx.x;
+  if (bid < 64) phase_gates(P, smem, bid, tid);
+  else phase_ainit(P, smem, 2048 + (bid - 64) * 16, 16, tid);
+}
+
+__global__ __launch_bounds__(256) void kL3(Params P) {
+  __shared__ float smem[256];
+  int bid = blockIdx.x, tid = threadIdx.x;
+  if (bid < 256) phase_scan1(P, smem, bid, tid);
+  else phase_ctx(P, smem, tid);
+}
+
+__global__ __launch_bounds__(256) void kL4(Params P) {
+  __shared__ float smem[8];
+  int bid = blockIdx.x, tid = threadIdx.x;
+  if (bid < 128) phase_mix(P, smem, 0, P.A, P.A2, DK0.a, DK0.b, bid * 32, 32, tid);
+  else phase_scan2(P, bid - 128, tid);
+}
+
+__global__ __launch_bounds__(256) void kL5(Params P) {
+  __shared__ float smem[2120];
+  int bid = blockIdx.x, tid = threadIdx.x;
+  if (bid < 128) phase_mix(P, smem, 1, P.A2, P.A, DK1.a, DK1.b, bid * 32, 32, tid);
+  else phase_ygemm(P, smem, bid - 128, tid);
+}
+
+__global__ __launch_bounds__(256) void kL6(Params P) {
+  __shared__ float smem[8];
+  int bid = blockIdx.x, tid = threadIdx.x;
+  phase_mix(P, smem, 2, P.A, P.A2, DK2.a, DK2.b, bid * 16, 16, tid);
+}
+
+__global__ __launch_bounds__(256) void kL7(Params P) {
+  __shared__ float smem[2112];
+  phase_horner(P, smem, P.A2, P.YH + 2 * 8192, 0, P.YH + 8192, P.R1,
+               blockIdx.x, threadIdx.x);
+}
+__global__ __launch_bounds__(256) void kL8(Params P) {
+  __shared__ float smem[2112];
+  phase_horner(P, smem, P.A2, P.R1, 8192, P.YH, P.R2, blockIdx.x, threadIdx.x);
+}
+__global__ __launch_bounds__(256) void kL9(Params P) {
+  __shared__ float smem[2112];
+  phase_horner(P, smem, P.A2, P.R2, 8192, nullptr, P.R1, blockIdx.x,
+               threadIdx.x);
+}
+
+__global__ __launch_bounds__(256) void kL10(Params P) {
+  __shared__ float smem[276];
+  phase_findec(P, smem, blockIdx.x, threadIdx.x);
+}
+
+constexpr size_t O_PS = 0;
+constexpr size_t O_DS = 65536;
+constexpr size_t O_HGG = 69632;
+constexpr size_t O_HGS = 73728;
+constexpr size_t O_HGA = 77824;
+constexpr size_t O_FG = 81920;
+constexpr size_t O_CTX = 86016;
+constexpr size_t O_V = 86336;
+constexpr size_t O_SV = 90432;
+constexpr size_t O_U = 90496;
+constexpr size_t O_PF = 123264;
+constexpr size_t O_QF = 647552;
+constexpr size_t O_PB = 1171840;
+constexpr size_t O_QB = 1696128;
+constexpr size_t O_LF = 2220416;
+constexpr size_t O_LB = 2285952;
+constexpr size_t O_YH = 2351488;
+constexpr size_t O_R1 = 2376064;
+constexpr size_t O_R2 = 2507136;
+constexpr size_t O_GM = 2638208;
+constexpr size_t O_GLV = 2642304;
+constexpr size_t O_A = 2646400;
+constexpr size_t O_A2 = 3694976;
 
 }
 
@@ -653,93 +692,82 @@
                               void* d_out, int out_size, void* d_ws,
                               size_t ws_size, hipStream_t stream) {
   (void)in_sizes; (void)n_in; (void)out_size; (void)ws_size;
-  const float* x = (const float*)d_in[0];
-  const float* gW1 = (const float*)d_in[1];
-  const float* gb1 = (const float*)d_in[2];
-  const float* g_ln_w = (const float*)d_in[3];
-  const float* g_ln_b = (const float*)d_in[4];
-  const float* gW2 = (const float*)d_in[5];
-  const float* gb2 = (const float*)d_in[6];
-  const float* sW1 = (const float*)d_in[7];
-  const float* sb1 = (const float*)d_in[8];
-  const float* sW2 = (const float*)d_in[9];
-  const float* sb2 = (const float*)d_in[10];
-  const float* aW1 = (const float*)d_in[11];
-  const float* ab1 = (const float*)d_in[12];
-  const float* aW2 = (const float*)d_in[13];
-  const float* ab2 = (const float*)d_in[14];
-  const float* g2f = (const float*)d_in[18];
-  const float* sector_emb = (const float*)d_in[19];
-  const float* asset_emb = (const float*)d_in[20];
-  const float* decay_f = (const float*)d_in[21];
-  const float* decay_b = (const float*)d_in[22];
-  const float* tW = (const float*)d_in[23];
-  const float* tb = (const float*)d_in[24];
-  const float* psi = (const float*)d_in[25];
-  const float* log_sigma = (const float*)d_in[26];
-  const float* step_logits = (const float*)d_in[27];
-  const float* noise_scale = (const float*)d_in[28];
-  const float* Wk = (const float*)d_in[29];
-  const float* mean_w = (const float*)d_in[30];
-  const float* mean_b = (const float*)d_in[31];
-  const float* lv_w = (const float*)d_in[32];
-  const float* lv_b = (const float*)d_in[33];
-  const float* dW1 = (const float*)d_in[34];
-  const float* db1 = (const float*)d_in[35];
-  const float* d_ln_w = (const float*)d_in[36];
-  const float* d_ln_b = (const float*)d_in[37];
-  const float* mW = (const float*)d_in[38];
-  const float* mb = (const float*)d_in[39];
-  const float* lvW = (const float*)d_in[40];
-  const float* lvb = (const float*)d_in[41];
-  float* out = (float*)d_out;
   float* w = (float*)d_ws;
-
-  const uint32_t dka[3] = {DK0.a, DK1.a, DK2.a};
-  const uint32_t dkb[3] = {DK0.b, DK1.b, DK2.b};
+  Params prm;
+  prm.x = (const float*)d_in[0];
+  prm.gW1 = (const float*)d_in[1];
+  prm.gb1 = (const float*)d_in[2];
+  prm.glnw = (const float*)d_in[3];
+  prm.glnb = (const float*)d_in[4];
+  prm.gW2 = (const float*)d_in[5];
+  prm.gb2 = (const float*)d_in[6];
+  prm.sW1 = (const float*)d_in[7];
+  prm.sb1 = (const float*)d_in[8];
+  prm.sW2 = (const float*)d_in[9];
+  prm.sb2 = (const float*)d_in[10];
+  prm.aW1 = (const float*)d_in[11];
+  prm.ab1 = (const float*)d_in[12];
+  prm.aW2 = (const float*)d_in[13];
+  prm.ab2 = (const float*)d_in[14];
+  prm.g2f = (const float*)d_in[18];
+  prm.semb = (const float*)d_in[19];
+  prm.aemb = (const float*)d_in[20];
+  prm.decay_f = (const float*)d_in[21];
+  prm.decay_b = (const float*)d_in[22];
+  prm.tW = (const float*)d_in[23];
+  prm.tb = (const float*)d_in[24];
+  prm.psi = (const float*)d_in[25];
+  prm.log_sigma = (const float*)d_in[26];
+  prm.step_logits = (const float*)d_in[27];
+  prm.noise_scale = (const float*)d_in[28];
+  prm.Wk = (const float*)d_in[29];
+  prm.mean_w = (const float*)d_in[30];
+  prm.mean_b = (const float*)d_in[31];
+  prm.lv_w = (const float*)d_in[32];
+  prm.lv_b = (const float*)d_in[33];
+  prm.dW1 = (const float*)d_in[34];
+  prm.db1 = (const float*)d_in[35];
+  prm.dlnw = (const float*)d_in[36];
+  prm.dlnb = (const float*)d_in[37];
+  prm.mW = (const float*)d_in[38];
+  prm.mb = (const float*)d_in[39];
+  prm.lvW = (const float*)d_in[40];
+  prm.lvb = (const float*)d_in[41];
+  prm.out = (float*)d_out;
+  prm.ps = w + O_PS;
+  prm.ds = w + O_DS;
+  prm.hgG = w + O_HGG;
+  prm.hgS = w + O_HGS;
+  prm.hgA = w + O_HGA;
+  prm.fg = w + O_FG;
+  prm.ctx = w + O_CTX;
+  prm.v = w + O_V;
+  prm.sv = w + O_SV;
+  prm.u = w + O_U;
+  prm.Pf = w + O_PF;
+  prm.Qf = w + O_QF;
+  prm.Pb = w + O_PB;
+  prm.Qb = w + O_QB;
+  prm.Lf = w + O_LF;
+  prm.Lb = w + O_LB;
+  prm.YH = w + O_YH;
+  prm.R1 = w + O_R1;
+  prm.R2 = w + O_R2;
+  prm.gm = w + O_GM;
+  prm.glv = w + O_GLV;
+  prm.A = w + O_A;
+  prm.A2 = w + O_A2;
 
   hipMemsetAsync(w + O_SV, 0, 64 * sizeof(float), stream);
-
-  k_reduce_x<<<256, 256, 0, stream>>>(x, w + O_PS);
-  k_combine<<<16, 256, 0, stream>>>(x, w + O_PS, w + O_SM, w + O_DS);
-  k_hidden<<<48, 256, 0, stream>>>(w + O_SM, w + O_DS, gW1, gb1, g_ln_w,
-                                   g_ln_b, sW1, sb1, aW1, ab1, w + O_HGG,
-                                   w + O_HGS, w + O_HGA);
-  k_s2<<<dim3(16, 8), 192, 0, stream>>>(w + O_HGS, sW2, sb2, sector_emb,
-                                        w + O_SG);
-  k_a2<<<dim3(16, 4), 256, 0, stream>>>(w + O_HGA, aW2, ab2, asset_emb,
-                                        w + O_AG);
-  k_fgate<<<16, 256, 0, stream>>>(w + O_HGG, gW2, gb2, g2f, w + O_SG, w + O_AG,
-                                  w + O_FG);
-  k_ctx<<<1, 256, 0, stream>>>(w + O_FG, w + O_CTX);
-
-  k_a_init<<<4096, 256, 0, stream>>>(psi, log_sigma, w + O_A);
-  const size_t asrc[3] = {O_A, O_A2, O_A};
-  const size_t adst[3] = {O_A2, O_A, O_A2};
-  for (int s = 0; s < 3; ++s) {
-    k_mix_sym<<<4096, 256, 0, stream>>>(w + asrc[s], w + adst[s], w + O_CTX,
-                                        step_logits, noise_scale, s, dka[s],
-                                        dkb[s]);
-  }
-
-  k_vcompute<<<32, 256, 0, stream>>>(Wk, mean_w, lv_w, w + O_V, w + O_SV);
-  k_scan1<<<256, 256, 0, stream>>>(x, w + O_FG, decay_f, decay_b, w + O_V,
-                                   w + O_PF, w + O_QF, w + O_PB, w + O_QB,
-                                   w + O_LF, w + O_LB);
-  k_scan2<<<128, 256, 0, stream>>>(w + O_PF, w + O_QF, w + O_PB, w + O_QB,
-                                   w + O_LF, w + O_LB, decay_f, decay_b,
-                                   w + O_U);
-  k_ygemm<<<dim3(8, 4), 256, 0, stream>>>(w + O_U, tW, tb, w + O_SV, mean_b,
-                                          lv_b, w + O_GM, w + O_GLV, w + O_YH);
-
-  k_horner<<<dim3(8, 16), 256, 0, stream>>>(w + O_A2, w + O_YH + 2 * 8192, 0,
-                                            w + O_YH + 1 * 8192, w + O_R1);
-  k_horner<<<dim3(8, 16), 256, 0, stream>>>(w + O_A2, w + O_R1, 8192, w + O_YH,
-                                            w + O_R2);
-  k_horner<<<dim3(8, 16), 256, 0, stream>>>(w + O_A2, w + O_R2, 8192, nullptr,
-                                            w + O_R1);
-  k_final<<<16, 256, 0, stream>>>(w + O_R1, w + O_GM, w + O_GLV);
-
-  k_decoder<<<16, 128, 0, stream>>>(w + O_GM, w + O_GLV, dW1, db1, d_ln_w,
-                                    d_ln_b, mW, mb, lvW, lvb, out);
-}
+  kL0<<<256, 256, 0, stream>>>(prm);
+  kL1<<<208, 256, 0, stream>>>(prm);
+  kL2<<<192, 256, 0, stream>>>(prm);
+  kL3<<<257, 256, 0, stream>>>(prm);
+  kL4<<<256, 256, 0, stream>>>(prm);
+  kL5<<<160, 256, 0, stream>>>(prm);
+  kL6<<<256, 256, 0, stream>>>(prm);
+  kL7<<<128, 256, 0, stream>>>(prm);
+  kL8<<<128, 256, 0, stream>>>(prm);
+  kL9<<<128, 256, 0, stream>>>(prm);
+  kL10<<<16, 256, 0, stream>>>(prm);
+}
```

Result: slower. 409.6 us (+14.2%).
